# Kernel tuning notes

Hardware: AMD Instinct MI355X
Metric: run time of the kernel (lower is better)

The kernel has to match this reference:

```python
import jax, jax.numpy as jnp
import numpy as np

B, L, D = 4, 1024, 256
HD = 16                 # head_dim
H = D // HD             # num heads = 16
DI = 2 * D              # mamba d_inner (expand=2) = 512
S = 64                  # d_state
KC = 4                  # d_conv
DTR = max(1, D // 16)   # dt_rank = 16
SCALES = (1, 2, 4, 8)


def _lin_interp(x, L_out):
    # F.interpolate(mode='linear', align_corners=False) on (B, L_in, D)
    L_in = x.shape[1]
    pos = (jnp.arange(L_out, dtype=x.dtype) + 0.5) * (L_in / L_out) - 0.5
    pos = jnp.clip(pos, 0.0, L_in - 1)
    lo = jnp.floor(pos).astype(jnp.int32)
    hi = jnp.minimum(lo + 1, L_in - 1)
    w = (pos - lo.astype(x.dtype))[None, :, None]
    return x[:, lo] * (1.0 - w) + x[:, hi] * w


def setup_inputs() -> dict:
    key = jax.random.key(0)
    ks = jax.random.split(key, 24)
    sc = 0.02
    inp = {
        "x": jax.random.normal(ks[0], (B, L, D), jnp.float32),
        "ln_g": jnp.ones((D,), jnp.float32),
        "ln_b": jnp.zeros((D,), jnp.float32),
        # MultiScaleQuery: 4 per-scale projections + fuse
        "mq_w": sc * jax.random.normal(ks[1], (4, D, D), jnp.float32),
        "mq_b": sc * jax.random.normal(ks[2], (4, D), jnp.float32),
        "fuse_w": sc * jax.random.normal(ks[3], (D, 4 * D), jnp.float32),
        "fuse_b": sc * jax.random.normal(ks[4], (D,), jnp.float32),
        # Mamba params
        "in_proj_w": sc * jax.random.normal(ks[5], (2 * DI, D), jnp.float32),
        "conv_w": 0.2 * jax.random.normal(ks[6], (DI, KC), jnp.float32),
        "conv_b": sc * jax.random.normal(ks[7], (DI,), jnp.float32),
        "x_proj_w": sc * jax.random.normal(ks[8], (DTR + 2 * S, DI), jnp.float32),
        "dt_w": sc * jax.random.normal(ks[9], (DI, DTR), jnp.float32),
        "dt_b": jnp.full((DI,), -4.0, jnp.float32),  # softplus -> small dt
        "A_log": jnp.log(jnp.tile(jnp.arange(1, S + 1, dtype=jnp.float32), (DI, 1))),
        "D_ssm": jnp.ones((DI,), jnp.float32),
        "out_w": sc * jax.random.normal(ks[10], (D, DI), jnp.float32),
        # StructuredSSD (q comes from MultiScaleQuery override; q_proj unused)
        "k_w": sc * jax.random.normal(ks[11], (D, D), jnp.float32),
        "k_b": sc * jax.random.normal(ks[12], (D,), jnp.float32),
        "v_w": sc * jax.random.normal(ks[13], (D, D), jnp.float32),
        "v_b": sc * jax.random.normal(ks[14], (D,), jnp.float32),
        "o_w": sc * jax.random.normal(ks[15], (D, D), jnp.float32),
        "o_b": sc * jax.random.normal(ks[16], (D,), jnp.float32),
        "log_tau": jnp.full((H,), np.log(16.0), jnp.float32),
        # Gate
        "gate_w": sc * jax.random.normal(ks[17], (D, 2 * D), jnp.float32),
        "gate_b": sc * jax.random.normal(ks[18], (D,), jnp.float32),
    }
    return inp


def reference(x, ln_g, ln_b, mq_w, mq_b, fuse_w, fuse_b,
              in_proj_w, conv_w, conv_b, x_proj_w, dt_w, dt_b,
              A_log, D_ssm, out_w,
              k_w, k_b, v_w, v_b, o_w, o_b, log_tau,
              gate_w, gate_b):
    Bsz, Lq, Dm = x.shape

    # ---- LayerNorm ----
    mu = x.mean(-1, keepdims=True)
    var = ((x - mu) ** 2).mean(-1, keepdims=True)
    xn = (x - mu) / jnp.sqrt(var + 1e-5) * ln_g + ln_b

    # ---- MultiScaleQuery ----
    qs = []
    for i, s in enumerate(SCALES):
        if s <= 1:
            q = xn @ mq_w[i].T + mq_b[i]
        else:
            xd = xn.reshape(Bsz, Lq // s, s, Dm).mean(2)   # avg_pool1d(k=s, stride=s)
            qd = xd @ mq_w[i].T + mq_b[i]
            q = _lin_interp(qd, Lq)
        qs.append(q)
    q = jnp.concatenate(qs, -1) @ fuse_w.T + fuse_b        # (B, L, D)

    # ---- Mamba (selective scan) ----
    xz = xn @ in_proj_w.T                                  # (B, L, 2*DI)
    xm, z = jnp.split(xz, 2, axis=-1)
    xp = jnp.pad(xm, ((0, 0), (KC - 1, 0), (0, 0)))        # causal depthwise conv
    xc = sum(xp[:, kk:kk + Lq, :] * conv_w[:, kk] for kk in range(KC)) + conv_b
    xc = jax.nn.silu(xc)                                   # (B, L, DI)
    dbc = xc @ x_proj_w.T                                  # (B, L, DTR+2S)
    dt_in, Bm, Cm = jnp.split(dbc, [DTR, DTR + S], axis=-1)
    dt = jax.nn.softplus(dt_in @ dt_w.T + dt_b)            # (B, L, DI)
    A = -jnp.exp(A_log)                                    # (DI, S)

    def step(h, inp):
        xt, dtt, Bt, Ct = inp                              # (B,DI) (B,DI) (B,S) (B,S)
        dA = jnp.exp(dtt[:, :, None] * A)                  # (B, DI, S)
        h = dA * h + (dtt * xt)[:, :, None] * Bt[:, None, :]
        y = jnp.einsum('bds,bs->bd', h, Ct)
        return h, y

    h0 = jnp.zeros((Bsz, DI, S), x.dtype)
    _, ys = jax.lax.scan(step, h0, (xc.transpose(1, 0, 2), dt.transpose(1, 0, 2),
                                    Bm.transpose(1, 0, 2), Cm.transpose(1, 0, 2)))
    y = ys.transpose(1, 0, 2) + xc * D_ssm                 # (B, L, DI)
    y = y * jax.nn.silu(z)
    ssm_out = y @ out_w.T                                  # (B, L, D)

    # ---- StructuredSSD (decay-masked attention, q override) ----
    k = xn @ k_w.T + k_b
    v = xn @ v_w.T + v_b
    hds = lambda t: t.reshape(Bsz, Lq, H, HD).transpose(0, 2, 1, 3)
    qh, kh, vh = hds(q), hds(k), hds(v)                    # (B, H, L, hd)
    scale = 1.0 / np.sqrt(HD)
    scores = jnp.einsum('bhqd,bhkd->bhqk', qh, kh) * scale
    idx = jnp.arange(Lq)
    dist = jnp.maximum(idx[:, None] - idx[None, :], 0).astype(x.dtype)
    tau = jnp.exp(log_tau)[:, None, None]                  # (H,1,1)
    mask = jnp.exp(-dist / tau)                            # (H, L, L); ==1 above diag
    scores = scores * mask
    denom = jnp.maximum(mask.sum(-1, keepdims=True), 1e-6)
    scores = scores / denom                                # broadcast over batch
    attn = jnp.einsum('bhqk,bhkd->bhqd', scores, vh)
    attn = attn.transpose(0, 2, 1, 3).reshape(Bsz, Lq, Dm)
    ssd_out = attn @ o_w.T + o_b

    # ---- Sigmoid gate fusion + residual ----
    gate = jax.nn.sigmoid(jnp.concatenate([ssm_out, ssd_out], -1) @ gate_w.T + gate_b)
    fused = gate * ssm_out + (1.0 - gate) * ssd_out
    return x + fused
```

## Files before the change

kernel.cpp:

```cpp
#include <hip/hip_runtime.h>
#include <math.h>

#define Bsz 4
#define Lseq 1024
#define Dm 256
#define Hh 16
#define HDm 16
#define DIm 512
#define Ssz 64
#define KCm 4
#define DTRm 16
#define NCH (Bsz * DIm)
#define CHK 64
#define NCHK (Lseq / CHK)
#define CHA 32
#define NCA (Lseq / CHA)

typedef __attribute__((ext_vector_type(8))) short s8v;
typedef __attribute__((ext_vector_type(4))) float f4v;

static __device__ __forceinline__ float wave_sum(float v) {
    #pragma unroll
    for (int m = 32; m >= 1; m >>= 1) v += __shfl_xor(v, m, 64);
    return v;
}

static __device__ __forceinline__ float bcast(float v, int l) {
    return __uint_as_float(__builtin_amdgcn_readlane(__float_as_uint(v), l));
}

static __device__ __forceinline__ short f2bf(float f) {
    unsigned int u = __float_as_uint(f);
    u = (u + 0x7fffu + ((u >> 16) & 1u)) >> 16;
    return (short)u;
}

static __device__ __forceinline__ s8v pack8(float4 a, float4 b) {
    s8v v;
    v[0] = f2bf(a.x); v[1] = f2bf(a.y); v[2] = f2bf(a.z); v[3] = f2bf(a.w);
    v[4] = f2bf(b.x); v[5] = f2bf(b.y); v[6] = f2bf(b.z); v[7] = f2bf(b.w);
    return v;
}

__global__ __launch_bounds__(256) void ln_kernel(const float* __restrict__ x,
                                                 const float* __restrict__ g,
                                                 const float* __restrict__ b,
                                                 float* __restrict__ xn) {
    int row = blockIdx.x;
    int tid = threadIdx.x;
    __shared__ float red[8];
    float v = x[(size_t)row * Dm + tid];
    float s = wave_sum(v);
    int wid = tid >> 6, lane = tid & 63;
    if (lane == 0) red[wid] = s;
    __syncthreads();
    float mean = (red[0] + red[1] + red[2] + red[3]) * (1.0f / Dm);
    float dv = v - mean;
    float s2 = wave_sum(dv * dv);
    if (lane == 0) red[4 + wid] = s2;
    __syncthreads();
    float var = (red[4] + red[5] + red[6] + red[7]) * (1.0f / Dm);
    float inv = rsqrtf(var + 1e-5f);
    xn[(size_t)row * Dm + tid] = dv * inv * g[tid] + b[tid];
}

__global__ void halve3_kernel(const float* __restrict__ xn, float* __restrict__ xd2,
                              float* __restrict__ xd4, float* __restrict__ xd8) {
    int idx = blockIdx.x * blockDim.x + threadIdx.x;
    if (idx < 524288) {
        int d = idx & 255, j = (idx >> 8) & 511, b = idx >> 17;
        const float* p = xn + ((size_t)(b * 1024 + 2 * j) * 256 + d);
        xd2[idx] = 0.5f * (p[0] + p[256]);
    } else if (idx < 786432) {
        int i = idx - 524288;
        int d = i & 255, j = (i >> 8) & 255, b = i >> 16;
        const float* p = xn + ((size_t)(b * 1024 + 4 * j) * 256 + d);
        xd4[i] = 0.25f * ((p[0] + p[256]) + (p[512] + p[768]));
    } else if (idx < 917504) {
        int i = idx - 786432;
        int d = i & 255, j = (i >> 8) & 127, b = i >> 15;
        const float* p = xn + ((size_t)(b * 1024 + 8 * j) * 256 + d);
        xd8[i] = 0.125f * (((p[0] + p[256]) + (p[512] + p[768]))
                         + ((p[1024] + p[1280]) + (p[1536] + p[1792])));
    }
}

__global__ __launch_bounds__(256) void conv_silu_kernel(const float* __restrict__ xm,
                                                        const float* __restrict__ cw,
                                                        const float* __restrict__ cb,
                                                        float* __restrict__ xc,
                                                        float* __restrict__ xcT) {
    __shared__ float tile[64][65];
    int blk = blockIdx.x;
    int cblk = blk & 7;
    int tblk = (blk >> 3) & 15;
    int b = blk >> 7;
    int c0 = cblk * 64, t0 = tblk * 64;
    int cc = threadIdx.x & 63;
    int tw = threadIdx.x >> 6;
    int c = c0 + cc;
    float w0 = cw[c * 4 + 0], w1 = cw[c * 4 + 1], w2 = cw[c * 4 + 2], w3 = cw[c * 4 + 3];
    float bias = cb[c];
    #pragma unroll 4
    for (int i = 0; i < 16; i++) {
        int tl = tw * 16 + i;
        int t = t0 + tl;
        const float* base = xm + ((size_t)(b * Lseq + t)) * DIm + c;
        float acc = bias + base[0] * w3;
        if (t >= 3) {
            acc += base[-3 * DIm] * w0 + base[-2 * DIm] * w1 + base[-1 * DIm] * w2;
        } else {
            if (t >= 1) acc += base[-1 * DIm] * w2;
            if (t >= 2) acc += base[-2 * DIm] * w1;
        }
        float r = acc / (1.0f + __expf(-acc));
        xc[((size_t)(b * Lseq + t)) * DIm + c] = r;
        tile[tl][cc] = r;
    }
    __syncthreads();
    int tcol = threadIdx.x & 63;
    int crow0 = threadIdx.x >> 6;
    #pragma unroll 4
    for (int j = 0; j < 16; j++) {
        int crow = crow0 * 16 + j;
        xcT[((size_t)(c0 + crow)) * (Bsz * Lseq) + b * Lseq + t0 + tcol] = tile[tcol][crow];
    }
}

__global__ __launch_bounds__(256) void proj8(const float* __restrict__ xn,
                                             const float* __restrict__ xd2,
                                             const float* __restrict__ xd4,
                                             const float* __restrict__ xd8,
                                             const float* __restrict__ in_proj_w,
                                             const float* __restrict__ k_w, const float* __restrict__ k_b,
                                             const float* __restrict__ v_w, const float* __restrict__ v_b,
                                             const float* __restrict__ mq_w, const float* __restrict__ mq_b,
                                             float* __restrict__ xm, float* __restrict__ zT,
                                             float* __restrict__ kmat, float* __restrict__ vmat,
                                             float* __restrict__ q0, float* __restrict__ qd2,
                                             float* __restrict__ qd4, float* __restrict__ qd8) {
    __shared__ unsigned short As[64][40];
    __shared__ unsigned short Ws[64][40];
    int bx = blockIdx.x;
    const float* A; const float* W; const float* bias; float* C;
    int ldc, transC = 0, n0, m0;
    if (bx < 512) {
        A = xn; W = in_proj_w; bias = nullptr; C = xm; ldc = DIm;
        n0 = (bx & 7) * 64; m0 = (bx >> 3) * 64;
    } else if (bx < 1024) {
        int l = bx - 512;
        A = xn; W = in_proj_w + 131072; bias = nullptr; C = zT; ldc = Bsz * Lseq; transC = 1;
        n0 = (l & 7) * 64; m0 = (l >> 3) * 64;
    } else if (bx < 1280) {
        int l = bx - 1024;
        A = xn; W = k_w; bias = k_b; C = kmat; ldc = Dm;
        n0 = (l & 3) * 64; m0 = (l >> 2) * 64;
    } else if (bx < 1536) {
        int l = bx - 1280;
        A = xn; W = v_w; bias = v_b; C = vmat; ldc = Dm;
        n0 = (l & 3) * 64; m0 = (l >> 2) * 64;
    } else if (bx < 1792) {
        int l = bx - 1536;
        A = xn; W = mq_w; bias = mq_b; C = q0; ldc = Dm;
        n0 = (l & 3) * 64; m0 = (l >> 2) * 64;
    } else if (bx < 1920) {
        int l = bx - 1792;
        A = xd2; W = mq_w + 65536; bias = mq_b + 256; C = qd2; ldc = Dm;
        n0 = (l & 3) * 64; m0 = (l >> 2) * 64;
    } else if (bx < 1984) {
        int l = bx - 1920;
        A = xd4; W = mq_w + 131072; bias = mq_b + 512; C = qd4; ldc = Dm;
        n0 = (l & 3) * 64; m0 = (l >> 2) * 64;
    } else {
        int l = bx - 1984;
        A = xd8; W = mq_w + 196608; bias = mq_b + 768; C = qd8; ldc = Dm;
        n0 = (l & 3) * 64; m0 = (l >> 2) * 64;
    }
    int tid = threadIdx.x;
    int wave = tid >> 6, lane = tid & 63;
    int quad = lane >> 4, r = lane & 15;
    int mo = (wave >> 1) * 32, no = (wave & 1) * 32;
    f4v acc[2][2];
    #pragma unroll
    for (int i = 0; i < 2; i++)
        #pragma unroll
        for (int j = 0; j < 2; j++) acc[i][j] = (f4v){0.f, 0.f, 0.f, 0.f};
    for (int k0 = 0; k0 < 256; k0 += 32) {
        {
            int m = tid >> 2, kk = (tid & 3) * 8;
            const float* ap = A + (size_t)(m0 + m) * 256 + k0 + kk;
            *(s8v*)&As[m][kk] = pack8(*(const float4*)ap, *(const float4*)(ap + 4));
        }
        {
            int n = tid >> 2, kk = (tid & 3) * 8;
            const float* wp = W + (size_t)(n0 + n) * 256 + k0 + kk;
            *(s8v*)&Ws[n][kk] = pack8(*(const float4*)wp, *(const float4*)(wp + 4));
        }
        __syncthreads();
        s8v af[2], bf[2];
        #pragma unroll
        for (int i = 0; i < 2; i++) af[i] = *(const s8v*)&As[mo + i * 16 + r][quad * 8];
        #pragma unroll
        for (int j = 0; j < 2; j++) bf[j] = *(const s8v*)&Ws[no + j * 16 + r][quad * 8];
        #pragma unroll
        for (int i = 0; i < 2; i++)
            #pragma unroll
            for (int j = 0; j < 2; j++)
                acc[i][j] = __builtin_amdgcn_mfma_f32_16x16x32_bf16(af[i], bf[j], acc[i][j], 0, 0, 0);
        __syncthreads();
    }
    #pragma unroll
    for (int i = 0; i < 2; i++)
        #pragma unroll
        for (int j = 0; j < 2; j++)
            #pragma unroll
            for (int reg = 0; reg < 4; reg++) {
                int m = m0 + mo + i * 16 + quad * 4 + reg;
                int n = n0 + no + j * 16 + r;
                float v = acc[i][j][reg];
                if (bias) v += bias[n];
                float* cp = transC ? (C + (size_t)n * ldc + m) : (C + (size_t)m * ldc + n);
                *cp = v;
            }
}

__global__ __launch_bounds__(256) void fuse_gemm(const float* __restrict__ q0,
                                                 const float* __restrict__ qd2,
                                                 const float* __restrict__ qd4,
                                                 const float* __restrict__ qd8,
                                                 const float* __restrict__ fuse_w,
                                                 const float* __restrict__ fuse_b,
                                                 float* __restrict__ qbuf) {
    __shared__ unsigned short As[64][40];
    __shared__ unsigned short Ws[64][40];
    int tid = threadIdx.x;
    int wave = tid >> 6, lane = tid & 63;
    int quad = lane >> 4, r = lane & 15;
    int m0 = blockIdx.y * 64, n0 = blockIdx.x * 64;
    int mo = (wave >> 1) * 32, no = (wave & 1) * 32;
    f4v acc[2][2];
    #pragma unroll
    for (int i = 0; i < 2; i++)
        #pragma unroll
        for (int j = 0; j < 2; j++) acc[i][j] = (f4v){0.f, 0.f, 0.f, 0.f};

    for (int k0 = 0; k0 < 1024; k0 += 32) {
        {
            int m = tid >> 2, kk = (tid & 3) * 8;
            int kg = k0 + kk;
            int seg = kg >> 8, dcol = kg & 255;
            int mg = m0 + m;
            s8v pv;
            if (seg == 0) {
                const float* ap = q0 + (size_t)mg * 256 + dcol;
                pv = pack8(*(const float4*)ap, *(const float4*)(ap + 4));
            } else {
                int t = mg & 1023, b = mg >> 10;
                int Lin = 512 >> (seg - 1);
                const float* qd = (seg == 1) ? qd2 : (seg == 2) ? qd4 : qd8;
                float pos = (t + 0.5f) * ((float)Lin / 1024.0f) - 0.5f;
                pos = fminf(fmaxf(pos, 0.0f), (float)(Lin - 1));
                int lo = (int)floorf(pos);
                int hi = min(lo + 1, Lin - 1);
                float w = pos - (float)lo;
                const float* plo = qd + ((size_t)(b * Lin + lo)) * 256 + dcol;
                const float* phi = qd + ((size_t)(b * Lin + hi)) * 256 + dcol;
                float4 l0 = *(const float4*)plo, l1 = *(const float4*)(plo + 4);
                float4 h0 = *(const float4*)phi, h1 = *(const float4*)(phi + 4);
                float4 r0, r1;
                r0.x = l0.x + w * (h0.x - l0.x); r0.y = l0.y + w * (h0.y - l0.y);
                r0.z = l0.z + w * (h0.z - l0.z); r0.w = l0.w + w * (h0.w - l0.w);
                r1.x = l1.x + w * (h1.x - l1.x); r1.y = l1.y + w * (h1.y - l1.y);
                r1.z = l1.z + w * (h1.z - l1.z); r1.w = l1.w + w * (h1.w - l1.w);
                pv = pack8(r0, r1);
            }
            *(s8v*)&As[m][kk] = pv;
        }
        {
            int n = tid >> 2, kk = (tid & 3) * 8;
            const float* wp = fuse_w + (size_t)(n0 + n) * 1024 + k0 + kk;
            *(s8v*)&Ws[n][kk] = pack8(*(const float4*)wp, *(const float4*)(wp + 4));
        }
        __syncthreads();
        s8v af[2], bf[2];
        #pragma unroll
        for (int i = 0; i < 2; i++) af[i] = *(const s8v*)&As[mo + i * 16 + r][quad * 8];
        #pragma unroll
        for (int j = 0; j < 2; j++) bf[j] = *(const s8v*)&Ws[no + j * 16 + r][quad * 8];
        #pragma unroll
        for (int i = 0; i < 2; i++)
            #pragma unroll
            for (int j = 0; j < 2; j++)
                acc[i][j] = __builtin_amdgcn_mfma_f32_16x16x32_bf16(af[i], bf[j], acc[i][j], 0, 0, 0);
        __syncthreads();
    }
    #pragma unroll
    for (int i = 0; i < 2; i++)
        #pragma unroll
        for (int j = 0; j < 2; j++)
            #pragma unroll
            for (int reg = 0; reg < 4; reg++) {
                int m = m0 + mo + i * 16 + quad * 4 + reg;
                int n = n0 + no + j * 16 + r;
                qbuf[(size_t)m * 256 + n] = acc[i][j][reg] + fuse_b[n];
            }
}

__global__ __launch_bounds__(256) void post2(const float* __restrict__ attn,
                                             const float* __restrict__ o_w,
                                             const float* __restrict__ o_b,
                                             const float* __restrict__ yT,
                                             const float* __restrict__ out_w,
                                             float* __restrict__ cat2) {
    __shared__ unsigned short As[64][40];
    __shared__ unsigned short Ws[64][40];
    int bx = blockIdx.x;
    const float* A; const float* W; const float* bias; float* C;
    int lda_m, lda_k, ldw, K, n0, m0;
    if (bx < 256) {
        A = attn; lda_m = 256; lda_k = 1; W = o_w; ldw = 256; bias = o_b;
        C = cat2 + 256; K = 256;
        n0 = (bx & 3) * 64; m0 = (bx >> 2) * 64;
    } else {
        int l = bx - 256;
        A = yT; lda_m = 1; lda_k = Bsz * Lseq; W = out_w; ldw = DIm; bias = nullptr;
        C = cat2; K = DIm;
        n0 = (l & 3) * 64; m0 = (l >> 2) * 64;
    }
    int tid = threadIdx.x;
    int wave = tid >> 6, lane = tid & 63;
    int quad = lane >> 4, r = lane & 15;
    int mo = (wave >> 1) * 32, no = (wave & 1) * 32;
    f4v acc[2][2];
    #pragma unroll
    for (int i = 0; i < 2; i++)
        #pragma unroll
        for (int j = 0; j < 2; j++) acc[i][j] = (f4v){0.f, 0.f, 0.f, 0.f};
    for (int k0 = 0; k0 < K; k0 += 32) {
        if (lda_k == 1) {
            int m = tid >> 2, kk = (tid & 3) * 8;
            const float* ap = A + (size_t)(m0 + m) * lda_m + k0 + kk;
            *(s8v*)&As[m][kk] = pack8(*(const float4*)ap, *(const float4*)(ap + 4));
        } else {
            int k = tid >> 3, m8 = (tid & 7) * 8;
            const float* ap = A + (size_t)(k0 + k) * lda_k + m0 + m8;
            float4 a0 = *(const float4*)ap;
            float4 a1 = *(const float4*)(ap + 4);
            float av[8] = {a0.x, a0.y, a0.z, a0.w, a1.x, a1.y, a1.z, a1.w};
            #pragma unroll
            for (int i = 0; i < 8; i++) As[m8 + i][k] = (unsigned short)f2bf(av[i]);
        }
        {
            int n = tid >> 2, kk = (tid & 3) * 8;
            const float* wp = W + (size_t)(n0 + n) * ldw + k0 + kk;
            *(s8v*)&Ws[n][kk] = pack8(*(const float4*)wp, *(const float4*)(wp + 4));
        }
        __syncthreads();
        s8v af[2], bf[2];
        #pragma unroll
        for (int i = 0; i < 2; i++) af[i] = *(const s8v*)&As[mo + i * 16 + r][quad * 8];
        #pragma unroll
        for (int j = 0; j < 2; j++) bf[j] = *(const s8v*)&Ws[no + j * 16 + r][quad * 8];
        #pragma unroll
        for (int i = 0; i < 2; i++)
            #pragma unroll
            for (int j = 0; j < 2; j++)
                acc[i][j] = __builtin_amdgcn_mfma_f32_16x16x32_bf16(af[i], bf[j], acc[i][j], 0, 0, 0);
        __syncthreads();
    }
    #pragma unroll
    for (int i = 0; i < 2; i++)
        #pragma unroll
        for (int j = 0; j < 2; j++)
            #pragma unroll
            for (int reg = 0; reg < 4; reg++) {
                int m = m0 + mo + i * 16 + quad * 4 + reg;
                int n = n0 + no + j * 16 + r;
                float v = acc[i][j][reg];
                if (bias) v += bias[n];
                C[(size_t)m * 512 + n] = v;
            }
}

__global__ __launch_bounds__(256) void gemm_bf16(const float* __restrict__ A, int lda_m, int lda_k,
                                                 const float* __restrict__ W, int ldw,
                                                 const float* __restrict__ bias,
                                                 float* __restrict__ C, int ldc,
                                                 int M, int N, int K, int accum, int transC,
                                                 const float* __restrict__ xres,
                                                 float* __restrict__ fout) {
    __shared__ unsigned short As[64][40];
    __shared__ unsigned short Ws[64][40];
    int tid = threadIdx.x;
    int wave = tid >> 6, lane = tid & 63;
    int quad = lane >> 4, r = lane & 15;
    int m0 = blockIdx.y * 64, n0 = blockIdx.x * 64;
    int mo = (wave >> 1) * 32, no = (wave & 1) * 32;
    f4v acc[2][2];
    #pragma unroll
    for (int i = 0; i < 2; i++)
        #pragma unroll
        for (int j = 0; j < 2; j++) acc[i][j] = (f4v){0.f, 0.f, 0.f, 0.f};

    for (int k0 = 0; k0 < K; k0 += 32) {
        if (lda_k == 1) {
            int m = tid >> 2, kk = (tid & 3) * 8;
            const float* ap = A + (size_t)(m0 + m) * lda_m + k0 + kk;
            *(s8v*)&As[m][kk] = pack8(*(const float4*)ap, *(const float4*)(ap + 4));
        } else {
            int k = tid >> 3, m8 = (tid & 7) * 8;
            const float* ap = A + (size_t)(k0 + k) * lda_k + m0 + m8;
            float4 a0 = *(const float4*)ap;
            float4 a1 = *(const float4*)(ap + 4);
            float av[8] = {a0.x, a0.y, a0.z, a0.w, a1.x, a1.y, a1.z, a1.w};
            #pragma unroll
            for (int i = 0; i < 8; i++) As[m8 + i][k] = (unsigned short)f2bf(av[i]);
        }
        {
            int n = tid >> 2, kk = (tid & 3) * 8;
            s8v pv;
            if (n0 + n < N) {
                const float* wp = W + (size_t)(n0 + n) * ldw + k0 + kk;
                pv = pack8(*(const float4*)wp, *(const float4*)(wp + 4));
            } else {
                pv = (s8v){0, 0, 0, 0, 0, 0, 0, 0};
            }
            *(s8v*)&Ws[n][kk] = pv;
        }
        __syncthreads();
        s8v af[2], bf[2];
        #pragma unroll
        for (int i = 0; i < 2; i++) af[i] = *(const s8v*)&As[mo + i * 16 + r][quad * 8];
        #pragma unroll
        for (int j = 0; j < 2; j++) bf[j] = *(const s8v*)&Ws[no + j * 16 + r][quad * 8];
        #pragma unroll
        for (int i = 0; i < 2; i++)
            #pragma unroll
            for (int j = 0; j < 2; j++)
                acc[i][j] = __builtin_amdgcn_mfma_f32_16x16x32_bf16(af[i], bf[j], acc[i][j], 0, 0, 0);
        __syncthreads();
    }
    #pragma unroll
    for (int i = 0; i < 2; i++)
        #pragma unroll
        for (int j = 0; j < 2; j++)
            #pragma unroll
            for (int reg = 0; reg < 4; reg++) {
                int m = m0 + mo + i * 16 + quad * 4 + reg;
                int n = n0 + no + j * 16 + r;
                if (n >= N) continue;
                float v = acc[i][j][reg];
                if (bias) v += bias[n];
                if (fout) {
                    float g = 1.0f / (1.0f + __expf(-v));
                    float ssm = A[(size_t)m * lda_m + n];
                    float ssd = A[(size_t)m * lda_m + 256 + n];
                    fout[(size_t)m * 256 + n] = xres[(size_t)m * 256 + n] + g * ssm + (1.0f - g) * ssd;
                } else {
                    float* cp = transC ? (C + (size_t)n * ldc + m) : (C + (size_t)m * ldc + n);
                    if (accum) v += *cp;
                    *cp = v;
                }
            }
}

__global__ __launch_bounds__(256) void gemm_f32(const float* __restrict__ A, int lda_m, int lda_k,
                                                const float* __restrict__ W, int ldw,
                                                const float* __restrict__ bias,
                                                float* __restrict__ C, int ldc,
                                                int M, int N, int K, int act, int accum, int transC) {
    __shared__ float As[16][72];
    __shared__ float Ws[16][72];
    int tid = threadIdx.x;
    int m0 = blockIdx.y * 64, n0 = blockIdx.x * 64;
    int tx = tid & 15, ty = tid >> 4;
    float acc[4][4] = {};
    for (int k0 = 0; k0 < K; k0 += 16) {
        {
            int ml = tid >> 2, kl = (tid & 3) * 4;
            const float4 av = *(const float4*)(A + (size_t)(m0 + ml) * lda_m + k0 + kl);
            As[kl + 0][ml] = av.x; As[kl + 1][ml] = av.y;
            As[kl + 2][ml] = av.z; As[kl + 3][ml] = av.w;
        }
        {
            int nl = tid >> 2, kl = (tid & 3) * 4;
            float4 wv;
            if (n0 + nl < N) wv = *(const float4*)(W + (size_t)(n0 + nl) * ldw + k0 + kl);
            else wv = make_float4(0.f, 0.f, 0.f, 0.f);
            Ws[kl + 0][nl] = wv.x; Ws[kl + 1][nl] = wv.y;
            Ws[kl + 2][nl] = wv.z; Ws[kl + 3][nl] = wv.w;
        }
        __syncthreads();
        #pragma unroll
        for (int kk = 0; kk < 16; kk++) {
            float4 av = *(const float4*)&As[kk][ty * 4];
            float4 bv = *(const float4*)&Ws[kk][tx * 4];
            float a[4] = {av.x, av.y, av.z, av.w};
            float bb[4] = {bv.x, bv.y, bv.z, bv.w};
            #pragma unroll
            for (int im = 0; im < 4; im++)
                #pragma unroll
                for (int in = 0; in < 4; in++)
                    acc[im][in] = fmaf(a[im], bb[in], acc[im][in]);
        }
        __syncthreads();
    }
    #pragma unroll
    for (int in = 0; in < 4; in++) {
        int n = n0 + tx * 4 + in;
        if (n >= N) continue;
        #pragma unroll
        for (int im = 0; im < 4; im++) {
            int m = m0 + ty * 4 + im;
            float v = acc[im][in];
            if (bias) v += bias[n];
            if (act == 1) v = fmaxf(v, 0.0f) + log1pf(expf(-fabsf(v)));
            float* cp = transC ? (C + (size_t)n * ldc + m) : (C + (size_t)m * ldc + n);
            if (accum) v += *cp;
            *cp = v;
        }
    }
}

__global__ __launch_bounds__(256) void scan_pass1(const float* __restrict__ xcT,
                                                  const float* __restrict__ dtmT,
                                                  const float* __restrict__ dbc,
                                                  const float* __restrict__ A_log,
                                                  float* __restrict__ hloc,
                                                  float* __restrict__ Pc) {
    int wave = blockIdx.x * 4 + (threadIdx.x >> 6);
    int lane = threadIdx.x & 63;
    int ch = wave & (NCH - 1);
    int c  = wave >> 11;
    int b = ch >> 9, d = ch & (DIm - 1);
    float As = -__expf(A_log[d * Ssz + lane]);
    int base_m = b * Lseq + c * CHK;
    float dt_vec = dtmT[(size_t)d * (Bsz * Lseq) + base_m + lane];
    float x_vec  = xcT [(size_t)d * (Bsz * Lseq) + base_m + lane];
    float ux = dt_vec * x_vec;
    float S = dt_vec;
    #pragma unroll
    for (int m = 1; m < 64; m <<= 1) {
        float o = __shfl_up(S, m, 64);
        if (lane >= m) S += o;
    }
    float Stot = bcast(S, 63);
    const float* Bp = dbc + (size_t)base_m * 144 + DTRm + lane;
    float h0 = 0.f, h1 = 0.f, h2 = 0.f, h3 = 0.f;
    #pragma unroll 4
    for (int t = 0; t < CHK; t += 4) {
        float B0 = Bp[0], B1 = Bp[144], B2 = Bp[288], B3 = Bp[432];
        Bp += 576;
        float w0 = __expf(As * (Stot - bcast(S, t)))     * bcast(ux, t);
        float w1 = __expf(As * (Stot - bcast(S, t + 1))) * bcast(ux, t + 1);
        float w2 = __expf(As * (Stot - bcast(S, t + 2))) * bcast(ux, t + 2);
        float w3 = __expf(As * (Stot - bcast(S, t + 3))) * bcast(ux, t + 3);
        h0 = fmaf(w0, B0, h0); h1 = fmaf(w1, B1, h1);
        h2 = fmaf(w2, B2, h2); h3 = fmaf(w3, B3, h3);
    }
    size_t o = ((size_t)ch * NCHK + c) * Ssz + lane;
    hloc[o] = (h0 + h1) + (h2 + h3);
    Pc[o] = __expf(As * Stot);
}

__global__ __launch_bounds__(256) void scan_combine(const float* __restrict__ hloc,
                                                    const float* __restrict__ Pc,
                                                    float* __restrict__ Hinit) {
    int wave = blockIdx.x * 4 + (threadIdx.x >> 6);
    int lane = threadIdx.x & 63;
    size_t base = (size_t)wave * NCHK * Ssz + lane;
    float H = 0.0f;
    #pragma unroll
    for (int c = 0; c < NCHK; c++) {
        size_t o = base + (size_t)c * Ssz;
        Hinit[o] = H;
        H = fmaf(Pc[o], H, hloc[o]);
    }
}

__global__ __launch_bounds__(256) void scan_pass3(const float* __restrict__ xcT,
                                                  const float* __restrict__ dtmT,
                                                  const float* __restrict__ zT,
                                                  const float* __restrict__ dbc,
                                                  const float* __restrict__ A_log,
                                                  const float* __restrict__ D_ssm,
                                                  const float* __restrict__ Hinit,
                                                  float* __restrict__ yT) {
    __shared__ float hCs[4][16][68];
    int wid = threadIdx.x >> 6;
    int lane = threadIdx.x & 63;
    int wave = blockIdx.x * 4 + wid;
    int ch = wave & (NCH - 1);
    int c  = wave >> 11;
    int b = ch >> 9, d = ch & (DIm - 1);
    float As = -__expf(A_log[d * Ssz + lane]);
    float Dd = D_ssm[d];
    int base_m = b * Lseq + c * CHK;
    float dt_vec = dtmT[(size_t)d * (Bsz * Lseq) + base_m + lane];
    float x_vec  = xcT [(size_t)d * (Bsz * Lseq) + base_m + lane];
    float zown   = zT  [(size_t)d * (Bsz * Lseq) + base_m + lane];
    float ux = dt_vec * x_vec;
    const float* Bp = dbc + (size_t)base_m * 144 + DTRm + lane;
    const float* Cp = Bp + Ssz;
    float h = Hinit[((size_t)ch * NCHK + c) * Ssz + lane];
    float yred = 0.0f;
    int tl = lane >> 2;
    int so = (lane & 3) * 16;
    for (int tb = 0; tb < 4; tb++) {
        #pragma unroll
        for (int j = 0; j < 16; j++) {
            int t = tb * 16 + j;
            float Bt = *Bp; Bp += 144;
            float Ct = *Cp; Cp += 144;
            float dtv = bcast(dt_vec, t);
            float u   = bcast(ux, t);
            float dA = __expf(dtv * As);
            h = fmaf(dA, h, u * Bt);
            hCs[wid][j][lane] = h * Ct;
        }
        const float* bp = &hCs[wid][tl][so];
        float4 a0 = *(const float4*)(bp + 0);
        float4 a1 = *(const float4*)(bp + 4);
        float4 a2 = *(const float4*)(bp + 8);
        float4 a3 = *(const float4*)(bp + 12);
        float part = ((a0.x + a0.y) + (a0.z + a0.w)) + ((a1.x + a1.y) + (a1.z + a1.w))
                   + ((a2.x + a2.y) + (a2.z + a2.w)) + ((a3.x + a3.y) + (a3.z + a3.w));
        part += __shfl_xor(part, 1, 64);
        part += __shfl_xor(part, 2, 64);
        float got = __shfl(part, ((lane - tb * 16) << 2) & 63, 64);
        if ((lane >> 4) == tb) yred = got;
    }
    float yg = (yred + x_vec * Dd) * (zown / (1.0f + __expf(-zown)));
    yT[(size_t)d * (Bsz * Lseq) + base_m + lane] = yg;
}

__global__ __launch_bounds__(256) void attn_p1(const float* __restrict__ k,
                                               const float* __restrict__ v,
                                               const float* __restrict__ log_tau,
                                               float* __restrict__ loc) {
    __shared__ float Ksh[4][CHA][20];
    __shared__ float Vsh[4][CHA][16];
    int wid = threadIdx.x >> 6, lane = threadIdx.x & 63;
    int wave = blockIdx.x * 4 + wid;
    int bh = wave >> 5;
    int c  = wave & 31;
    int b = bh >> 4, h = bh & 15;
    float inv_tau = __expf(-log_tau[h]);
    float rdec = __expf(-inv_tau);
    int t0 = c * CHA;
    int row = lane >> 1, hf = (lane & 1) * 8;
    const float* kp = k + ((size_t)(b * Lseq + t0 + row)) * Dm + h * HDm + hf;
    const float* vp = v + ((size_t)(b * Lseq + t0 + row)) * Dm + h * HDm + hf;
    *(float4*)&Ksh[wid][row][hf]     = *(const float4*)kp;
    *(float4*)&Ksh[wid][row][hf + 4] = *(const float4*)(kp + 4);
    *(float4*)&Vsh[wid][row][hf]     = *(const float4*)vp;
    *(float4*)&Vsh[wid][row][hf + 4] = *(const float4*)(vp + 4);
    int g = lane >> 4, cc = lane & 15;
    float4 U = {0.f, 0.f, 0.f, 0.f}, T = {0.f, 0.f, 0.f, 0.f};
    #pragma unroll 8
    for (int s = 0; s < CHA; s++) {
        float4 kf = *(const float4*)&Ksh[wid][s][4 * g];
        float vv = Vsh[wid][s][cc];
        float u0 = kf.x * vv, u1 = kf.y * vv, u2 = kf.z * vv, u3 = kf.w * vv;
        U.x += u0; U.y += u1; U.z += u2; U.w += u3;
        T.x = fmaf(rdec, T.x, u0); T.y = fmaf(rdec, T.y, u1);
        T.z = fmaf(rdec, T.z, u2); T.w = fmaf(rdec, T.w, u3);
    }
    float* op = loc + ((size_t)bh * NCA + c) * 512;
    *(float4*)(op + lane * 4) = U;
    *(float4*)(op + 256 + lane * 4) = T;
}

__global__ __launch_bounds__(256) void attn_p2(const float* __restrict__ loc,
                                               const float* __restrict__ log_tau,
                                               float* __restrict__ init,
                                               float* __restrict__ kvtot) {
    int bh = blockIdx.x, e = threadIdx.x;
    float inv_tau = __expf(-log_tau[bh & 15]);
    float rp = __expf(-(float)CHA * inv_tau);
    const float* lp = loc + (size_t)bh * NCA * 512;
    float* ip = init + (size_t)bh * NCA * 512;
    float Ua = 0.f, Ta = 0.f;
    #pragma unroll 8
    for (int c = 0; c < NCA; c++) {
        ip[c * 512 + e] = Ua;
        Ua += lp[c * 512 + e];
        ip[c * 512 + 256 + e] = Ta;
        Ta = fmaf(rp, Ta, lp[c * 512 + 256 + e]);
    }
    kvtot[bh * 256 + e] = Ua;
}

__global__ __launch_bounds__(256) void attn_p3(const float* __restrict__ q,
                                               const float* __restrict__ k,
                                               const float* __restrict__ v,
                                               const float* __restrict__ log_tau,
                                               const float* __restrict__ init,
                                               const float* __restrict__ kvtot,
                                               float* __restrict__ out) {
    __shared__ float Ksh[4][CHA][20];
    __shared__ float Qsh[4][CHA][20];
    __shared__ float Vsh[4][CHA][16];
    __shared__ float Ysh[4][CHA][16];
    int wid = threadIdx.x >> 6, lane = threadIdx.x & 63;
    int wave = blockIdx.x * 4 + wid;
    int bh = wave >> 5;
    int c  = wave & 31;
    int b = bh >> 4, h = bh & 15;
    float inv_tau = __expf(-log_tau[h]);
    float rdec = __expf(-inv_tau);
    int t0 = c * CHA;
    int row = lane >> 1, hf = (lane & 1) * 8;
    const float* kp = k + ((size_t)(b * Lseq + t0 + row)) * Dm + h * HDm + hf;
    const float* vp = v + ((size_t)(b * Lseq + t0 + row)) * Dm + h * HDm + hf;
    const float* qp = q + ((size_t)(b * Lseq + t0 + row)) * Dm + h * HDm + hf;
    *(float4*)&Ksh[wid][row][hf]     = *(const float4*)kp;
    *(float4*)&Ksh[wid][row][hf + 4] = *(const float4*)(kp + 4);
    *(float4*)&Vsh[wid][row][hf]     = *(const float4*)vp;
    *(float4*)&Vsh[wid][row][hf + 4] = *(const float4*)(vp + 4);
    *(float4*)&Qsh[wid][row][hf]     = *(const float4*)qp;
    *(float4*)&Qsh[wid][row][hf + 4] = *(const float4*)(qp + 4);
    int g = lane >> 4, cc = lane & 15;
    size_t ibase = ((size_t)bh * NCA + c) * 512;
    float4 U  = *(const float4*)(init + ibase + lane * 4);
    float4 T  = *(const float4*)(init + ibase + 256 + lane * 4);
    float4 KV = *(const float4*)(kvtot + bh * 256 + lane * 4);
    float om = 1.0f - rdec;
    float geom = (om > 1e-8f) ? (1.0f - __expf(-inv_tau * (float)t0)) / om : (float)t0;
    #pragma unroll 4
    for (int s = 0; s < CHA; s++) {
        int i = t0 + s;
        geom = fmaf(geom, rdec, 1.0f);
        float4 kf = *(const float4*)&Ksh[wid][s][4 * g];
        float4 qf = *(const float4*)&Qsh[wid][s][4 * g];
        float vv = Vsh[wid][s][cc];
        float u0 = kf.x * vv, u1 = kf.y * vv, u2 = kf.z * vv, u3 = kf.w * vv;
        U.x += u0; U.y += u1; U.z += u2; U.w += u3;
        T.x = fmaf(rdec, T.x, u0); T.y = fmaf(rdec, T.y, u1);
        T.z = fmaf(rdec, T.z, u2); T.w = fmaf(rdec, T.w, u3);
        float p;
        p = qf.x * (KV.x - U.x + T.x);
        p = fmaf(qf.y, KV.y - U.y + T.y, p);
        p = fmaf(qf.z, KV.z - U.z + T.z, p);
        p = fmaf(qf.w, KV.w - U.w + T.w, p);
        p += __shfl_xor(p, 16, 64);
        p += __shfl_xor(p, 32, 64);
        float deno = fmaxf((float)(Lseq - 1 - i) + geom, 1e-6f);
        float yv = p * (0.25f / deno);
        if (lane < 16) Ysh[wid][s][lane] = yv;
    }
    float* op = out + ((size_t)(b * Lseq + t0 + row)) * Dm + h * HDm + hf;
    *(float4*)op       = *(const float4*)&Ysh[wid][row][hf];
    *(float4*)(op + 4) = *(const float4*)&Ysh[wid][row][hf + 4];
}

extern "C" void kernel_launch(void* const* d_in, const int* in_sizes, int n_in,
                              void* d_out, int out_size, void* d_ws, size_t ws_size,
                              hipStream_t stream) {
    const float* x        = (const float*)d_in[0];
    const float* ln_g     = (const float*)d_in[1];
    const float* ln_b     = (const float*)d_in[2];
    const float* mq_w     = (const float*)d_in[3];
    const float* mq_b     = (const float*)d_in[4];
    const float* fuse_w   = (const float*)d_in[5];
    const float* fuse_b   = (const float*)d_in[6];
    const float* in_proj_w= (const float*)d_in[7];
    const float* conv_w   = (const float*)d_in[8];
    const float* conv_b   = (const float*)d_in[9];
    const float* x_proj_w = (const float*)d_in[10];
    const float* dt_w     = (const float*)d_in[11];
    const float* dt_b     = (const float*)d_in[12];
    const float* A_log    = (const float*)d_in[13];
    const float* D_ssm    = (const float*)d_in[14];
    const float* out_w    = (const float*)d_in[15];
    const float* k_w      = (const float*)d_in[16];
    const float* k_b      = (const float*)d_in[17];
    const float* v_w      = (const float*)d_in[18];
    const float* v_b      = (const float*)d_in[19];
    const float* o_w      = (const float*)d_in[20];
    const float* o_b      = (const float*)d_in[21];
    const float* log_tau  = (const float*)d_in[22];
    const float* gate_w   = (const float*)d_in[23];
    const float* gate_b   = (const float*)d_in[24];
    float* outp = (float*)d_out;

    const int M = Bsz * Lseq;
    float* ws = (float*)d_ws;
    size_t off = 0;
    float* xn    = ws + off; off += (size_t)M * Dm;
    float* xm    = ws + off; off += (size_t)M * DIm;
    float* zT    = ws + off; off += (size_t)DIm * M;
    float* xcT   = ws + off; off += (size_t)DIm * M;
    float* dbc   = ws + off; off += (size_t)M * 144;
    float* dtmT  = ws + off; off += (size_t)DIm * M;
    float* yT    = ws + off; off += (size_t)DIm * M;
    float* xd2   = ws + off; off += (size_t)Bsz * 512 * Dm;
    float* xd4   = ws + off; off += (size_t)Bsz * 256 * Dm;
    float* xd8   = ws + off; off += (size_t)Bsz * 128 * Dm;
    float* qd2   = ws + off; off += (size_t)Bsz * 512 * Dm;
    float* qd4   = ws + off; off += (size_t)Bsz * 256 * Dm;
    float* qd8   = ws + off; off += (size_t)Bsz * 128 * Dm;
    float* qcat  = ws + off; off += (size_t)M * 4 * Dm;
    float* qbuf  = ws + off; off += (size_t)M * Dm;
    float* kmat  = ws + off; off += (size_t)M * Dm;
    float* vmat  = ws + off; off += (size_t)M * Dm;
    float* attn  = ws + off; off += (size_t)M * Dm;
    float* cat2  = ws + off; off += (size_t)M * 2 * Dm;
    float* xc    = cat2;
    float* q0    = qcat;

    ln_kernel<<<M, 256, 0, stream>>>(x, ln_g, ln_b, xn);

    halve3_kernel<<<(917504 + 255) / 256, 256, 0, stream>>>(xn, xd2, xd4, xd8);

    proj8<<<2016, 256, 0, stream>>>(xn, xd2, xd4, xd8, in_proj_w,
        k_w, k_b, v_w, v_b, mq_w, mq_b,
        xm, zT, kmat, vmat, q0, qd2, qd4, qd8);

    fuse_gemm<<<dim3(4, 64), 256, 0, stream>>>(q0, qd2, qd4, qd8, fuse_w, fuse_b, qbuf);

    conv_silu_kernel<<<512, 256, 0, stream>>>(xm, conv_w, conv_b, xc, xcT);

    gemm_bf16<<<dim3(3, 64), 256, 0, stream>>>(xc, DIm, 1, x_proj_w, DIm,
        nullptr, dbc, 144, M, 144, DIm, 0, 0, nullptr, nullptr);

    gemm_f32<<<dim3(8, 64), 256, 0, stream>>>(dbc, 144, 1, dt_w, DTRm,
        dt_b, dtmT, M, M, DIm, DTRm, 1, 0, 1);

    float* aloc  = qcat;
    float* ainit = qcat + (size_t)64 * NCA * 512;
    float* kvtot = qcat + (size_t)2 * 64 * NCA * 512;
    attn_p1<<<512, 256, 0, stream>>>(kmat, vmat, log_tau, aloc);
    attn_p2<<<64, 256, 0, stream>>>(aloc, log_tau, ainit, kvtot);
    attn_p3<<<512, 256, 0, stream>>>(qbuf, kmat, vmat, log_tau, ainit, kvtot, attn);

    float* hloc  = qcat;
    float* Pc    = qcat + (size_t)NCH * NCHK * Ssz;
    float* Hinit = qbuf;
    scan_pass1<<<(NCH * NCHK) / 4, 256, 0, stream>>>(xcT, dtmT, dbc, A_log, hloc, Pc);
    scan_combine<<<NCH / 4, 256, 0, stream>>>(hloc, Pc, Hinit);
    scan_pass3<<<(NCH * NCHK) / 4, 256, 0, stream>>>(xcT, dtmT, zT, dbc, A_log, D_ssm, Hinit, yT);

    post2<<<512, 256, 0, stream>>>(attn, o_w, o_b, yT, out_w, cat2);

    gemm_bf16<<<dim3(4, 64), 256, 0, stream>>>(cat2, 2 * Dm, 1, gate_w, 2 * Dm,
        gate_b, nullptr, 0, M, Dm, 2 * Dm, 0, 0, x, outp);
}
```

Before: 365.0 us.

## Merge independent stages into horizontally fused kernels to cut launches

Fuses layernorm with multiscale average pooling in one kernel. It then packs independent stages into shared launches by block-index ranges: fuse GEMM with conv+SiLU, x_proj GEMM with attention pass 1, dt GEMM with attention pass 2, and scan pass 1 with attention pass 3. The attention chunk size is halved and the scan combine writes back in place. The aim is fewer kernel launches and better overlap of small independent stages, at the cost of heterogeneous blocks inside each kernel and reused workspace aliasing that must stay race-free.

```diff
diff --git a/kernel.cpp b/kernel.cpp
--- a/kernel.cpp
+++ b/kernel.cpp
@@ -13,7 +13,7 @@
 #define NCH (Bsz * DIm)
 #define CHK 64
 #define NCHK (Lseq / CHK)
-#define CHA 32
+#define CHA 16
 #define NCA (Lseq / CHA)
 
 typedef __attribute__((ext_vector_type(8))) short s8v;
@@ -42,88 +42,57 @@
     return v;
 }
 
-__global__ __launch_bounds__(256) void ln_kernel(const float* __restrict__ x,
-                                                 const float* __restrict__ g,
-                                                 const float* __restrict__ b,
-                                                 float* __restrict__ xn) {
-    int row = blockIdx.x;
-    int tid = threadIdx.x;
-    __shared__ float red[8];
-    float v = x[(size_t)row * Dm + tid];
-    float s = wave_sum(v);
-    int wid = tid >> 6, lane = tid & 63;
-    if (lane == 0) red[wid] = s;
+__global__ __launch_bounds__(256) void ln_pool(const float* __restrict__ x,
+                                               const float* __restrict__ g,
+                                               const float* __restrict__ bb,
+                                               float* __restrict__ xn, float* __restrict__ xd2,
+                                               float* __restrict__ xd4, float* __restrict__ xd8) {
+    __shared__ float p2[4][256];
+    int wid = threadIdx.x >> 6, lane = threadIdx.x & 63;
+    int gr0 = blockIdx.x * 8;
+    int b = gr0 >> 10, t0 = gr0 & 1023;
+    float4 g4 = *(const float4*)(g + lane * 4);
+    float4 b4 = *(const float4*)(bb + lane * 4);
+    float4 res[2];
+    #pragma unroll
+    for (int rr = 0; rr < 2; rr++) {
+        int row = gr0 + wid * 2 + rr;
+        float4 xv = *(const float4*)(x + (size_t)row * 256 + lane * 4);
+        float s = wave_sum(xv.x + xv.y + xv.z + xv.w);
+        float mean = s * (1.0f / 256.0f);
+        float d0 = xv.x - mean, d1 = xv.y - mean, d2 = xv.z - mean, d3 = xv.w - mean;
+        float s2 = wave_sum(d0 * d0 + d1 * d1 + d2 * d2 + d3 * d3);
+        float inv = rsqrtf(s2 * (1.0f / 256.0f) + 1e-5f);
+        float4 r;
+        r.x = d0 * inv * g4.x + b4.x; r.y = d1 * inv * g4.y + b4.y;
+        r.z = d2 * inv * g4.z + b4.z; r.w = d3 * inv * g4.w + b4.w;
+        *(float4*)(xn + (size_t)row * 256 + lane * 4) = r;
+        res[rr] = r;
+    }
+    float4 a2;
+    a2.x = 0.5f * (res[0].x + res[1].x); a2.y = 0.5f * (res[0].y + res[1].y);
+    a2.z = 0.5f * (res[0].z + res[1].z); a2.w = 0.5f * (res[0].w + res[1].w);
+    *(float4*)(xd2 + (size_t)(b * 512 + (t0 >> 1) + wid) * 256 + lane * 4) = a2;
+    *(float4*)&p2[wid][lane * 4] = a2;
     __syncthreads();
-    float mean = (red[0] + red[1] + red[2] + red[3]) * (1.0f / Dm);
-    float dv = v - mean;
-    float s2 = wave_sum(dv * dv);
-    if (lane == 0) red[4 + wid] = s2;
-    __syncthreads();
-    float var = (red[4] + red[5] + red[6] + red[7]) * (1.0f / Dm);
-    float inv = rsqrtf(var + 1e-5f);
-    xn[(size_t)row * Dm + tid] = dv * inv * g[tid] + b[tid];
-}
-
-__global__ void halve3_kernel(const float* __restrict__ xn, float* __restrict__ xd2,
-                              float* __restrict__ xd4, float* __restrict__ xd8) {
-    int idx = blockIdx.x * blockDim.x + threadIdx.x;
-    if (idx < 524288) {
-        int d = idx & 255, j = (idx >> 8) & 511, b = idx >> 17;
-        const float* p = xn + ((size_t)(b * 1024 + 2 * j) * 256 + d);
-        xd2[idx] = 0.5f * (p[0] + p[256]);
-    } else if (idx < 786432) {
-        int i = idx - 524288;
-        int d = i & 255, j = (i >> 8) & 255, b = i >> 16;
-        const float* p = xn + ((size_t)(b * 1024 + 4 * j) * 256 + d);
-        xd4[i] = 0.25f * ((p[0] + p[256]) + (p[512] + p[768]));
-    } else if (idx < 917504) {
-        int i = idx - 786432;
-        int d = i & 255, j = (i >> 8) & 127, b = i >> 15;
-        const float* p = xn + ((size_t)(b * 1024 + 8 * j) * 256 + d);
-        xd8[i] = 0.125f * (((p[0] + p[256]) + (p[512] + p[768]))
-                         + ((p[1024] + p[1280]) + (p[1536] + p[1792])));
-    }
-}
-
-__global__ __launch_bounds__(256) void conv_silu_kernel(const float* __restrict__ xm,
-                                                        const float* __restrict__ cw,
-                                                        const float* __restrict__ cb,
-                                                        float* __restrict__ xc,
-                                                        float* __restrict__ xcT) {
-    __shared__ float tile[64][65];
-    int blk = blockIdx.x;
-    int cblk = blk & 7;
-    int tblk = (blk >> 3) & 15;
-    int b = blk >> 7;
-    int c0 = cblk * 64, t0 = tblk * 64;
-    int cc = threadIdx.x & 63;
-    int tw = threadIdx.x >> 6;
-    int c = c0 + cc;
-    float w0 = cw[c * 4 + 0], w1 = cw[c * 4 + 1], w2 = cw[c * 4 + 2], w3 = cw[c * 4 + 3];
-    float bias = cb[c];
-    #pragma unroll 4
-    for (int i = 0; i < 16; i++) {
-        int tl = tw * 16 + i;
-        int t = t0 + tl;
-        const float* base = xm + ((size_t)(b * Lseq + t)) * DIm + c;
-        float acc = bias + base[0] * w3;
-        if (t >= 3) {
-            acc += base[-3 * DIm] * w0 + base[-2 * DIm] * w1 + base[-1 * DIm] * w2;
-        } else {
-            if (t >= 1) acc += base[-1 * DIm] * w2;
-            if (t >= 2) acc += base[-2 * DIm] * w1;
-        }
-        float r = acc / (1.0f + __expf(-acc));
-        xc[((size_t)(b * Lseq + t)) * DIm + c] = r;
-        tile[tl][cc] = r;
-    }
-    __syncthreads();
-    int tcol = threadIdx.x & 63;
-    int crow0 = threadIdx.x >> 6;
-    #pragma unroll 4
-    for (int j = 0; j < 16; j++) {
-        int crow = crow0 * 16 + j;
-        xcT[((size_t)(c0 + crow)) * (Bsz * Lseq) + b * Lseq + t0 + tcol] = tile[tcol][crow];
+    if (wid < 2) {
+        float4 u = *(const float4*)&p2[2 * wid][lane * 4];
+        float4 w = *(const float4*)&p2[2 * wid + 1][lane * 4];
+        float4 m;
+        m.x = 0.5f * (u.x + w.x); m.y = 0.5f * (u.y + w.y);
+        m.z = 0.5f * (u.z + w.z); m.w = 0.5f * (u.w + w.w);
+        *(float4*)(xd4 + (size_t)(b * 256 + (t0 >> 2) + wid) * 256 + lane * 4) = m;
+    } else if (wid == 2) {
+        float4 q0 = *(const float4*)&p2[0][lane * 4];
+        float4 q1 = *(const float4*)&p2[1][lane * 4];
+        float4 q2 = *(const float4*)&p2[2][lane * 4];
+        float4 q3 = *(const float4*)&p2[3][lane * 4];
+        float4 m;
+        m.x = 0.25f * ((q0.x + q1.x) + (q2.x + q3.x));
+        m.y = 0.25f * ((q0.y + q1.y) + (q2.y + q3.y));
+        m.z = 0.25f * ((q0.z + q1.z) + (q2.z + q3.z));
+        m.w = 0.25f * ((q0.w + q1.w) + (q2.w + q3.w));
+        *(float4*)(xd8 + (size_t)(b * 128 + (t0 >> 3)) * 256 + lane * 4) = m;
     }
 }
 
@@ -224,269 +193,250 @@
             }
 }
 
-__global__ __launch_bounds__(256) void fuse_gemm(const float* __restrict__ q0,
-                                                 const float* __restrict__ qd2,
-                                                 const float* __restrict__ qd4,
-                                                 const float* __restrict__ qd8,
-                                                 const float* __restrict__ fuse_w,
-                                                 const float* __restrict__ fuse_b,
-                                                 float* __restrict__ qbuf) {
-    __shared__ unsigned short As[64][40];
-    __shared__ unsigned short Ws[64][40];
+__global__ __launch_bounds__(256) void mid2(const float* __restrict__ q0,
+                                            const float* __restrict__ qd2,
+                                            const float* __restrict__ qd4,
+                                            const float* __restrict__ qd8,
+                                            const float* __restrict__ fuse_w,
+                                            const float* __restrict__ fuse_b,
+                                            float* __restrict__ qbuf,
+                                            const float* __restrict__ xm,
+                                            const float* __restrict__ cw,
+                                            const float* __restrict__ cb,
+                                            float* __restrict__ xc, float* __restrict__ xcT) {
+    __shared__ __align__(16) char smem[16640];
+    int bx = blockIdx.x;
     int tid = threadIdx.x;
-    int wave = tid >> 6, lane = tid & 63;
-    int quad = lane >> 4, r = lane & 15;
-    int m0 = blockIdx.y * 64, n0 = blockIdx.x * 64;
-    int mo = (wave >> 1) * 32, no = (wave & 1) * 32;
-    f4v acc[2][2];
-    #pragma unroll
-    for (int i = 0; i < 2; i++)
-        #pragma unroll
-        for (int j = 0; j < 2; j++) acc[i][j] = (f4v){0.f, 0.f, 0.f, 0.f};
-
-    for (int k0 = 0; k0 < 1024; k0 += 32) {
-        {
-            int m = tid >> 2, kk = (tid & 3) * 8;
-            int kg = k0 + kk;
-            int seg = kg >> 8, dcol = kg & 255;
-            int mg = m0 + m;
-            s8v pv;
-            if (seg == 0) {
-                const float* ap = q0 + (size_t)mg * 256 + dcol;
-                pv = pack8(*(const float4*)ap, *(const float4*)(ap + 4));
+    if (bx < 256) {
+        unsigned short (*As)[40] = (unsigned short(*)[40])smem;
+        unsigned short (*Ws)[40] = (unsigned short(*)[40])(smem + 5120);
+        int wave = tid >> 6, lane = tid & 63;
+        int quad = lane >> 4, r = lane & 15;
+        int n0 = (bx & 3) * 64, m0 = (bx >> 2) * 64;
+        int mo = (wave >> 1) * 32, no = (wave & 1) * 32;
+        f4v acc[2][2];
+        #pragma unroll
+        for (int i = 0; i < 2; i++)
+            #pragma unroll
+            for (int j = 0; j < 2; j++) acc[i][j] = (f4v){0.f, 0.f, 0.f, 0.f};
+        for (int k0 = 0; k0 < 1024; k0 += 32) {
+            {
+                int m = tid >> 2, kk = (tid & 3) * 8;
+                int kg = k0 + kk;
+                int seg = kg >> 8, dcol = kg & 255;
+                int mg = m0 + m;
+                s8v pv;
+                if (seg == 0) {
+                    const float* ap = q0 + (size_t)mg * 256 + dcol;
+                    pv = pack8(*(const float4*)ap, *(const float4*)(ap + 4));
+                } else {
+                    int t = mg & 1023, b = mg >> 10;
+                    int Lin = 512 >> (seg - 1);
+                    const float* qd = (seg == 1) ? qd2 : (seg == 2) ? qd4 : qd8;
+                    float pos = (t + 0.5f) * ((float)Lin / 1024.0f) - 0.5f;
+                    pos = fminf(fmaxf(pos, 0.0f), (float)(Lin - 1));
+                    int lo = (int)floorf(pos);
+                    int hi = min(lo + 1, Lin - 1);
+                    float w = pos - (float)lo;
+                    const float* plo = qd + ((size_t)(b * Lin + lo)) * 256 + dcol;
+                    const float* phi = qd + ((size_t)(b * Lin + hi)) * 256 + dcol;
+                    float4 l0 = *(const float4*)plo, l1 = *(const float4*)(plo + 4);
+                    float4 h0 = *(const float4*)phi, h1 = *(const float4*)(phi + 4);
+                    float4 r0, r1;
+                    r0.x = l0.x + w * (h0.x - l0.x); r0.y = l0.y + w * (h0.y - l0.y);
+                    r0.z = l0.z + w * (h0.z - l0.z); r0.w = l0.w + w * (h0.w - l0.w);
+                    r1.x = l1.x + w * (h1.x - l1.x); r1.y = l1.y + w * (h1.y - l1.y);
+                    r1.z = l1.z + w * (h1.z - l1.z); r1.w = l1.w + w * (h1.w - l1.w);
+                    pv = pack8(r0, r1);
+                }
+                *(s8v*)&As[m][kk] = pv;
+            }
+            {
+                int n = tid >> 2, kk = (tid & 3) * 8;
+                const float* wp = fuse_w + (size_t)(n0 + n) * 1024 + k0 + kk;
+                *(s8v*)&Ws[n][kk] = pack8(*(const float4*)wp, *(const float4*)(wp + 4));
+            }
+            __syncthreads();
+            s8v af[2], bf[2];
+            #pragma unroll
+            for (int i = 0; i < 2; i++) af[i] = *(const s8v*)&As[mo + i * 16 + r][quad * 8];
+            #pragma unroll
+            for (int j = 0; j < 2; j++) bf[j] = *(const s8v*)&Ws[no + j * 16 + r][quad * 8];
+            #pragma unroll
+            for (int i = 0; i < 2; i++)
+                #pragma unroll
+                for (int j = 0; j < 2; j++)
+                    acc[i][j] = __builtin_amdgcn_mfma_f32_16x16x32_bf16(af[i], bf[j], acc[i][j], 0, 0, 0);
+            __syncthreads();
+        }
+        #pragma unroll
+        for (int i = 0; i < 2; i++)
+            #pragma unroll
+            for (int j = 0; j < 2; j++)
+                #pragma unroll
+                for (int reg = 0; reg < 4; reg++) {
+                    int m = m0 + mo + i * 16 + quad * 4 + reg;
+                    int n = n0 + no + j * 16 + r;
+                    qbuf[(size_t)m * 256 + n] = acc[i][j][reg] + fuse_b[n];
+                }
+    } else {
+        float (*tile)[65] = (float(*)[65])smem;
+        int blk = bx - 256;
+        int cblk = blk & 7;
+        int tblk = (blk >> 3) & 15;
+        int b = blk >> 7;
+        int c0 = cblk * 64, t0 = tblk * 64;
+        int cc = tid & 63;
+        int tw = tid >> 6;
+        int c = c0 + cc;
+        float w0 = cw[c * 4 + 0], w1 = cw[c * 4 + 1], w2 = cw[c * 4 + 2], w3 = cw[c * 4 + 3];
+        float bias = cb[c];
+        #pragma unroll 4
+        for (int i = 0; i < 16; i++) {
+            int tl = tw * 16 + i;
+            int t = t0 + tl;
+            const float* base = xm + ((size_t)(b * Lseq + t)) * DIm + c;
+            float acc = bias + base[0] * w3;
+            if (t >= 3) {
+                acc += base[-3 * DIm] * w0 + base[-2 * DIm] * w1 + base[-1 * DIm] * w2;
             } else {
-                int t = mg & 1023, b = mg >> 10;
-                int Lin = 512 >> (seg - 1);
-                const float* qd = (seg == 1) ? qd2 : (seg == 2) ? qd4 : qd8;
-                float pos = (t + 0.5f) * ((float)Lin / 1024.0f) - 0.5f;
-                pos = fminf(fmaxf(pos, 0.0f), (float)(Lin - 1));
-                int lo = (int)floorf(pos);
-                int hi = min(lo + 1, Lin - 1);
-                float w = pos - (float)lo;
-                const float* plo = qd + ((size_t)(b * Lin + lo)) * 256 + dcol;
-                const float* phi = qd + ((size_t)(b * Lin + hi)) * 256 + dcol;
-                float4 l0 = *(const float4*)plo, l1 = *(const float4*)(plo + 4);
-                float4 h0 = *(const float4*)phi, h1 = *(const float4*)(phi + 4);
-                float4 r0, r1;
-                r0.x = l0.x + w * (h0.x - l0.x); r0.y = l0.y + w * (h0.y - l0.y);
-                r0.z = l0.z + w * (h0.z - l0.z); r0.w = l0.w + w * (h0.w - l0.w);
-                r1.x = l1.x + w * (h1.x - l1.x); r1.y = l1.y + w * (h1.y - l1.y);
-                r1.z = l1.z + w * (h1.z - l1.z); r1.w = l1.w + w * (h1.w - l1.w);
-                pv = pack8(r0, r1);
+                if (t >= 1) acc += base[-1 * DIm] * w2;
+                if (t >= 2) acc += base[-2 * DIm] * w1;
             }
-            *(s8v*)&As[m][kk] = pv;
-        }
-        {
-            int n = tid >> 2, kk = (tid & 3) * 8;
-            const float* wp = fuse_w + (size_t)(n0 + n) * 1024 + k0 + kk;
-            *(s8v*)&Ws[n][kk] = pack8(*(const float4*)wp, *(const float4*)(wp + 4));
+            float r = acc / (1.0f + __expf(-acc));
+            xc[((size_t)(b * Lseq + t)) * DIm + c] = r;
+            tile[tl][cc] = r;
         }
         __syncthreads();
-        s8v af[2], bf[2];
-        #pragma unroll
-        for (int i = 0; i < 2; i++) af[i] = *(const s8v*)&As[mo + i * 16 + r][quad * 8];
-        #pragma unroll
-        for (int j = 0; j < 2; j++) bf[j] = *(const s8v*)&Ws[no + j * 16 + r][quad * 8];
+        int tcol = tid & 63;
+        int crow0 = tid >> 6;
+        #pragma unroll 4
+        for (int j = 0; j < 16; j++) {
+            int crow = crow0 * 16 + j;
+            xcT[((size_t)(c0 + crow)) * (Bsz * Lseq) + b * Lseq + t0 + tcol] = tile[tcol][crow];
+        }
+    }
+}
+
+__global__ __launch_bounds__(256) void xproj_ap1(const float* __restrict__ xc,
+                                                 const float* __restrict__ x_proj_w,
+                                                 float* __restrict__ dbc,
+                                                 const float* __restrict__ kmat,
+                                                 const float* __restrict__ vmat,
+                                                 const float* __restrict__ log_tau,
+                                                 float* __restrict__ loc) {
+    __shared__ __align__(16) char smem[10240];
+    int bx = blockIdx.x;
+    int tid = threadIdx.x;
+    int wid = tid >> 6, lane = tid & 63;
+    if (bx < 192) {
+        unsigned short (*As)[40] = (unsigned short(*)[40])smem;
+        unsigned short (*Ws)[40] = (unsigned short(*)[40])(smem + 5120);
+        int quad = lane >> 4, r = lane & 15;
+        int n0 = (bx % 3) * 64, m0 = (bx / 3) * 64;
+        int mo = (wid >> 1) * 32, no = (wid & 1) * 32;
+        f4v acc[2][2];
         #pragma unroll
         for (int i = 0; i < 2; i++)
             #pragma unroll
+            for (int j = 0; j < 2; j++) acc[i][j] = (f4v){0.f, 0.f, 0.f, 0.f};
+        for (int k0 = 0; k0 < 512; k0 += 32) {
+            {
+                int m = tid >> 2, kk = (tid & 3) * 8;
+                const float* ap = xc + (size_t)(m0 + m) * 512 + k0 + kk;
+                *(s8v*)&As[m][kk] = pack8(*(const float4*)ap, *(const float4*)(ap + 4));
+            }
+            {
+                int n = tid >> 2, kk = (tid & 3) * 8;
+                s8v pv;
+                if (n0 + n < 144) {
+                    const float* wp = x_proj_w + (size_t)(n0 + n) * 512 + k0 + kk;
+                    pv = pack8(*(const float4*)wp, *(const float4*)(wp + 4));
+                } else {
+                    pv = (s8v){0, 0, 0, 0, 0, 0, 0, 0};
+                }
+                *(s8v*)&Ws[n][kk] = pv;
+            }
+            __syncthreads();
+            s8v af[2], bf[2];
+            #pragma unroll
+            for (int i = 0; i < 2; i++) af[i] = *(const s8v*)&As[mo + i * 16 + r][quad * 8];
+            #pragma unroll
+            for (int j = 0; j < 2; j++) bf[j] = *(const s8v*)&Ws[no + j * 16 + r][quad * 8];
+            #pragma unroll
+            for (int i = 0; i < 2; i++)
+                #pragma unroll
+                for (int j = 0; j < 2; j++)
+                    acc[i][j] = __builtin_amdgcn_mfma_f32_16x16x32_bf16(af[i], bf[j], acc[i][j], 0, 0, 0);
+            __syncthreads();
+        }
+        #pragma unroll
+        for (int i = 0; i < 2; i++)
+            #pragma unroll
             for (int j = 0; j < 2; j++)
-                acc[i][j] = __builtin_amdgcn_mfma_f32_16x16x32_bf16(af[i], bf[j], acc[i][j], 0, 0, 0);
-        __syncthreads();
-    }
-    #pragma unroll
-    for (int i = 0; i < 2; i++)
-        #pragma unroll
-        for (int j = 0; j < 2; j++)
-            #pragma unroll
-            for (int reg = 0; reg < 4; reg++) {
-                int m = m0 + mo + i * 16 + quad * 4 + reg;
-                int n = n0 + no + j * 16 + r;
-                qbuf[(size_t)m * 256 + n] = acc[i][j][reg] + fuse_b[n];
-            }
-}
-
-__global__ __launch_bounds__(256) void post2(const float* __restrict__ attn,
-                                             const float* __restrict__ o_w,
-                                             const float* __restrict__ o_b,
-                                             const float* __restrict__ yT,
-                                             const float* __restrict__ out_w,
-                                             float* __restrict__ cat2) {
-    __shared__ unsigned short As[64][40];
-    __shared__ unsigned short Ws[64][40];
+                #pragma unroll
+                for (int reg = 0; reg < 4; reg++) {
+                    int m = m0 + mo + i * 16 + quad * 4 + reg;
+                    int n = n0 + no + j * 16 + r;
+                    if (n >= 144) continue;
+                    dbc[(size_t)m * 144 + n] = acc[i][j][reg];
+                }
+    } else {
+        float (*Ksh)[CHA][20] = (float(*)[CHA][20])smem;
+        float (*Vsh)[CHA][16] = (float(*)[CHA][16])(smem + 5120);
+        int wv = (bx - 192) * 4 + wid;
+        int bh = wv >> 6, c = wv & 63;
+        int b = bh >> 4, h = bh & 15;
+        float inv_tau = __expf(-log_tau[h]);
+        float rdec = __expf(-inv_tau);
+        int t0 = c * CHA;
+        int row = lane >> 2, q4 = (lane & 3) * 4;
+        const float* kp = kmat + ((size_t)(b * Lseq + t0 + row)) * Dm + h * HDm + q4;
+        const float* vp = vmat + ((size_t)(b * Lseq + t0 + row)) * Dm + h * HDm + q4;
+        *(float4*)&Ksh[wid][row][q4] = *(const float4*)kp;
+        *(float4*)&Vsh[wid][row][q4] = *(const float4*)vp;
+        int g = lane >> 4, cc = lane & 15;
+        float4 U = {0.f, 0.f, 0.f, 0.f}, T = {0.f, 0.f, 0.f, 0.f};
+        #pragma unroll
+        for (int s = 0; s < CHA; s++) {
+            float4 kf = *(const float4*)&Ksh[wid][s][4 * g];
+            float vv = Vsh[wid][s][cc];
+            float u0 = kf.x * vv, u1 = kf.y * vv, u2 = kf.z * vv, u3 = kf.w * vv;
+            U.x += u0; U.y += u1; U.z += u2; U.w += u3;
+            T.x = fmaf(rdec, T.x, u0); T.y = fmaf(rdec, T.y, u1);
+            T.z = fmaf(rdec, T.z, u2); T.w = fmaf(rdec, T.w, u3);
+        }
+        float* op = loc + ((size_t)bh * NCA + c) * 512;
+        *(float4*)(op + lane * 4) = U;
+        *(float4*)(op + 256 + lane * 4) = T;
+    }
+}
+
+__global__ __launch_bounds__(256) void dt_ap2(const float* __restrict__ dbc,
+                                              const float* __restrict__ dt_w,
+                                              const float* __restrict__ dt_b,
+                                              float* __restrict__ dtmT,
+                                              float* __restrict__ loc,
+                                              const float* __restrict__ log_tau,
+                                              float* __restrict__ kvtot) {
+    __shared__ __align__(16) char smem[9216];
     int bx = blockIdx.x;
-    const float* A; const float* W; const float* bias; float* C;
-    int lda_m, lda_k, ldw, K, n0, m0;
-    if (bx < 256) {
-        A = attn; lda_m = 256; lda_k = 1; W = o_w; ldw = 256; bias = o_b;
-        C = cat2 + 256; K = 256;
-        n0 = (bx & 3) * 64; m0 = (bx >> 2) * 64;
-    } else {
-        int l = bx - 256;
-        A = yT; lda_m = 1; lda_k = Bsz * Lseq; W = out_w; ldw = DIm; bias = nullptr;
-        C = cat2; K = DIm;
-        n0 = (l & 3) * 64; m0 = (l >> 2) * 64;
-    }
     int tid = threadIdx.x;
-    int wave = tid >> 6, lane = tid & 63;
-    int quad = lane >> 4, r = lane & 15;
-    int mo = (wave >> 1) * 32, no = (wave & 1) * 32;
-    f4v acc[2][2];
-    #pragma unroll
-    for (int i = 0; i < 2; i++)
-        #pragma unroll
-        for (int j = 0; j < 2; j++) acc[i][j] = (f4v){0.f, 0.f, 0.f, 0.f};
-    for (int k0 = 0; k0 < K; k0 += 32) {
-        if (lda_k == 1) {
-            int m = tid >> 2, kk = (tid & 3) * 8;
-            const float* ap = A + (size_t)(m0 + m) * lda_m + k0 + kk;
-            *(s8v*)&As[m][kk] = pack8(*(const float4*)ap, *(const float4*)(ap + 4));
-        } else {
-            int k = tid >> 3, m8 = (tid & 7) * 8;
-            const float* ap = A + (size_t)(k0 + k) * lda_k + m0 + m8;
-            float4 a0 = *(const float4*)ap;
-            float4 a1 = *(const float4*)(ap + 4);
-            float av[8] = {a0.x, a0.y, a0.z, a0.w, a1.x, a1.y, a1.z, a1.w};
-            #pragma unroll
-            for (int i = 0; i < 8; i++) As[m8 + i][k] = (unsigned short)f2bf(av[i]);
-        }
-        {
-            int n = tid >> 2, kk = (tid & 3) * 8;
-            const float* wp = W + (size_t)(n0 + n) * ldw + k0 + kk;
-            *(s8v*)&Ws[n][kk] = pack8(*(const float4*)wp, *(const float4*)(wp + 4));
-        }
-        __syncthreads();
-        s8v af[2], bf[2];
-        #pragma unroll
-        for (int i = 0; i < 2; i++) af[i] = *(const s8v*)&As[mo + i * 16 + r][quad * 8];
-        #pragma unroll
-        for (int j = 0; j < 2; j++) bf[j] = *(const s8v*)&Ws[no + j * 16 + r][quad * 8];
-        #pragma unroll
-        for (int i = 0; i < 2; i++)
-            #pragma unroll
-            for (int j = 0; j < 2; j++)
-                acc[i][j] = __builtin_amdgcn_mfma_f32_16x16x32_bf16(af[i], bf[j], acc[i][j], 0, 0, 0);
-        __syncthreads();
-    }
-    #pragma unroll
-    for (int i = 0; i < 2; i++)
-        #pragma unroll
-        for (int j = 0; j < 2; j++)
-            #pragma unroll
-            for (int reg = 0; reg < 4; reg++) {
-                int m = m0 + mo + i * 16 + quad * 4 + reg;
-                int n = n0 + no + j * 16 + r;
-                float v = acc[i][j][reg];
-                if (bias) v += bias[n];
-                C[(size_t)m * 512 + n] = v;
-            }
-}
-
-__global__ __launch_bounds__(256) void gemm_bf16(const float* __restrict__ A, int lda_m, int lda_k,
-                                                 const float* __restrict__ W, int ldw,
-                                                 const float* __restrict__ bias,
-                                                 float* __restrict__ C, int ldc,
-                                                 int M, int N, int K, int accum, int transC,
-                                                 const float* __restrict__ xres,
-                                                 float* __restrict__ fout) {
-    __shared__ unsigned short As[64][40];
-    __shared__ unsigned short Ws[64][40];
-    int tid = threadIdx.x;
-    int wave = tid >> 6, lane = tid & 63;
-    int quad = lane >> 4, r = lane & 15;
-    int m0 = blockIdx.y * 64, n0 = blockIdx.x * 64;
-    int mo = (wave >> 1) * 32, no = (wave & 1) * 32;
-    f4v acc[2][2];
-    #pragma unroll
-    for (int i = 0; i < 2; i++)
-        #pragma unroll
-        for (int j = 0; j < 2; j++) acc[i][j] = (f4v){0.f, 0.f, 0.f, 0.f};
-
-    for (int k0 = 0; k0 < K; k0 += 32) {
-        if (lda_k == 1) {
-            int m = tid >> 2, kk = (tid & 3) * 8;
-            const float* ap = A + (size_t)(m0 + m) * lda_m + k0 + kk;
-            *(s8v*)&As[m][kk] = pack8(*(const float4*)ap, *(const float4*)(ap + 4));
-        } else {
-            int k = tid >> 3, m8 = (tid & 7) * 8;
-            const float* ap = A + (size_t)(k0 + k) * lda_k + m0 + m8;
-            float4 a0 = *(const float4*)ap;
-            float4 a1 = *(const float4*)(ap + 4);
-            float av[8] = {a0.x, a0.y, a0.z, a0.w, a1.x, a1.y, a1.z, a1.w};
-            #pragma unroll
-            for (int i = 0; i < 8; i++) As[m8 + i][k] = (unsigned short)f2bf(av[i]);
-        }
-        {
-            int n = tid >> 2, kk = (tid & 3) * 8;
-            s8v pv;
-            if (n0 + n < N) {
-                const float* wp = W + (size_t)(n0 + n) * ldw + k0 + kk;
-                pv = pack8(*(const float4*)wp, *(const float4*)(wp + 4));
-            } else {
-                pv = (s8v){0, 0, 0, 0, 0, 0, 0, 0};
-            }
-            *(s8v*)&Ws[n][kk] = pv;
-        }
-        __syncthreads();
-        s8v af[2], bf[2];
-        #pragma unroll
-        for (int i = 0; i < 2; i++) af[i] = *(const s8v*)&As[mo + i * 16 + r][quad * 8];
-        #pragma unroll
-        for (int j = 0; j < 2; j++) bf[j] = *(const s8v*)&Ws[no + j * 16 + r][quad * 8];
-        #pragma unroll
-        for (int i = 0; i < 2; i++)
-            #pragma unroll
-            for (int j = 0; j < 2; j++)
-                acc[i][j] = __builtin_amdgcn_mfma_f32_16x16x32_bf16(af[i], bf[j], acc[i][j], 0, 0, 0);
-        __syncthreads();
-    }
-    #pragma unroll
-    for (int i = 0; i < 2; i++)
-        #pragma unroll
-        for (int j = 0; j < 2; j++)
-            #pragma unroll
-            for (int reg = 0; reg < 4; reg++) {
-                int m = m0 + mo + i * 16 + quad * 4 + reg;
-                int n = n0 + no + j * 16 + r;
-                if (n >= N) continue;
-                float v = acc[i][j][reg];
-                if (bias) v += bias[n];
-                if (fout) {
-                    float g = 1.0f / (1.0f + __expf(-v));
-                    float ssm = A[(size_t)m * lda_m + n];
-                    float ssd = A[(size_t)m * lda_m + 256 + n];
-                    fout[(size_t)m * 256 + n] = xres[(size_t)m * 256 + n] + g * ssm + (1.0f - g) * ssd;
-                } else {
-                    float* cp = transC ? (C + (size_t)n * ldc + m) : (C + (size_t)m * ldc + n);
-                    if (accum) v += *cp;
-                    *cp = v;
-                }
-            }
-}
-
-__global__ __launch_bounds__(256) void gemm_f32(const float* __restrict__ A, int lda_m, int lda_k,
-                                                const float* __restrict__ W, int ldw,
-                                                const float* __restrict__ bias,
-                                                float* __restrict__ C, int ldc,
-                                                int M, int N, int K, int act, int accum, int transC) {
-    __shared__ float As[16][72];
-    __shared__ float Ws[16][72];
-    int tid = threadIdx.x;
-    int m0 = blockIdx.y * 64, n0 = blockIdx.x * 64;
-    int tx = tid & 15, ty = tid >> 4;
-    float acc[4][4] = {};
-    for (int k0 = 0; k0 < K; k0 += 16) {
+    if (bx < 512) {
+        float (*As)[72] = (float(*)[72])smem;
+        float (*Ws)[72] = (float(*)[72])(smem + 4608);
+        int m0 = (bx >> 3) * 64, n0 = (bx & 7) * 64;
+        int tx = tid & 15, ty = tid >> 4;
+        float acc[4][4] = {};
         {
             int ml = tid >> 2, kl = (tid & 3) * 4;
-            const float4 av = *(const float4*)(A + (size_t)(m0 + ml) * lda_m + k0 + kl);
+            const float4 av = *(const float4*)(dbc + (size_t)(m0 + ml) * 144 + kl);
             As[kl + 0][ml] = av.x; As[kl + 1][ml] = av.y;
             As[kl + 2][ml] = av.z; As[kl + 3][ml] = av.w;
         }
         {
             int nl = tid >> 2, kl = (tid & 3) * 4;
-            float4 wv;
-            if (n0 + nl < N) wv = *(const float4*)(W + (size_t)(n0 + nl) * ldw + k0 + kl);
-            else wv = make_float4(0.f, 0.f, 0.f, 0.f);
+            float4 wv = *(const float4*)(dt_w + (size_t)(n0 + nl) * 16 + kl);
             Ws[kl + 0][nl] = wv.x; Ws[kl + 1][nl] = wv.y;
             Ws[kl + 2][nl] = wv.z; Ws[kl + 3][nl] = wv.w;
         }
@@ -496,76 +446,147 @@
             float4 av = *(const float4*)&As[kk][ty * 4];
             float4 bv = *(const float4*)&Ws[kk][tx * 4];
             float a[4] = {av.x, av.y, av.z, av.w};
-            float bb[4] = {bv.x, bv.y, bv.z, bv.w};
+            float bbv[4] = {bv.x, bv.y, bv.z, bv.w};
             #pragma unroll
             for (int im = 0; im < 4; im++)
                 #pragma unroll
                 for (int in = 0; in < 4; in++)
-                    acc[im][in] = fmaf(a[im], bb[in], acc[im][in]);
-        }
-        __syncthreads();
-    }
-    #pragma unroll
-    for (int in = 0; in < 4; in++) {
-        int n = n0 + tx * 4 + in;
-        if (n >= N) continue;
-        #pragma unroll
-        for (int im = 0; im < 4; im++) {
-            int m = m0 + ty * 4 + im;
-            float v = acc[im][in];
-            if (bias) v += bias[n];
-            if (act == 1) v = fmaxf(v, 0.0f) + log1pf(expf(-fabsf(v)));
-            float* cp = transC ? (C + (size_t)n * ldc + m) : (C + (size_t)m * ldc + n);
-            if (accum) v += *cp;
-            *cp = v;
-        }
-    }
-}
-
-__global__ __launch_bounds__(256) void scan_pass1(const float* __restrict__ xcT,
-                                                  const float* __restrict__ dtmT,
-                                                  const float* __restrict__ dbc,
-                                                  const float* __restrict__ A_log,
-                                                  float* __restrict__ hloc,
-                                                  float* __restrict__ Pc) {
-    int wave = blockIdx.x * 4 + (threadIdx.x >> 6);
-    int lane = threadIdx.x & 63;
-    int ch = wave & (NCH - 1);
-    int c  = wave >> 11;
-    int b = ch >> 9, d = ch & (DIm - 1);
-    float As = -__expf(A_log[d * Ssz + lane]);
-    int base_m = b * Lseq + c * CHK;
-    float dt_vec = dtmT[(size_t)d * (Bsz * Lseq) + base_m + lane];
-    float x_vec  = xcT [(size_t)d * (Bsz * Lseq) + base_m + lane];
-    float ux = dt_vec * x_vec;
-    float S = dt_vec;
-    #pragma unroll
-    for (int m = 1; m < 64; m <<= 1) {
-        float o = __shfl_up(S, m, 64);
-        if (lane >= m) S += o;
-    }
-    float Stot = bcast(S, 63);
-    const float* Bp = dbc + (size_t)base_m * 144 + DTRm + lane;
-    float h0 = 0.f, h1 = 0.f, h2 = 0.f, h3 = 0.f;
-    #pragma unroll 4
-    for (int t = 0; t < CHK; t += 4) {
-        float B0 = Bp[0], B1 = Bp[144], B2 = Bp[288], B3 = Bp[432];
-        Bp += 576;
-        float w0 = __expf(As * (Stot - bcast(S, t)))     * bcast(ux, t);
-        float w1 = __expf(As * (Stot - bcast(S, t + 1))) * bcast(ux, t + 1);
-        float w2 = __expf(As * (Stot - bcast(S, t + 2))) * bcast(ux, t + 2);
-        float w3 = __expf(As * (Stot - bcast(S, t + 3))) * bcast(ux, t + 3);
-        h0 = fmaf(w0, B0, h0); h1 = fmaf(w1, B1, h1);
-        h2 = fmaf(w2, B2, h2); h3 = fmaf(w3, B3, h3);
-    }
-    size_t o = ((size_t)ch * NCHK + c) * Ssz + lane;
-    hloc[o] = (h0 + h1) + (h2 + h3);
-    Pc[o] = __expf(As * Stot);
-}
-
-__global__ __launch_bounds__(256) void scan_combine(const float* __restrict__ hloc,
-                                                    const float* __restrict__ Pc,
-                                                    float* __restrict__ Hinit) {
+                    acc[im][in] = fmaf(a[im], bbv[in], acc[im][in]);
+        }
+        #pragma unroll
+        for (int in = 0; in < 4; in++) {
+            int n = n0 + tx * 4 + in;
+            #pragma unroll
+            for (int im = 0; im < 4; im++) {
+                int m = m0 + ty * 4 + im;
+                float v = acc[im][in] + dt_b[n];
+                v = fmaxf(v, 0.0f) + log1pf(expf(-fabsf(v)));
+                dtmT[(size_t)n * (Bsz * Lseq) + m] = v;
+            }
+        }
+    } else {
+        int bh = bx - 512, e = tid;
+        float inv_tau = __expf(-log_tau[bh & 15]);
+        float rp = __expf(-(float)CHA * inv_tau);
+        float* lp = loc + (size_t)bh * NCA * 512;
+        float Ua = 0.f, Ta = 0.f;
+        #pragma unroll 8
+        for (int c = 0; c < NCA; c++) {
+            float tu = lp[c * 512 + e];
+            lp[c * 512 + e] = Ua;
+            Ua += tu;
+            float tt = lp[c * 512 + 256 + e];
+            lp[c * 512 + 256 + e] = Ta;
+            Ta = fmaf(rp, Ta, tt);
+        }
+        kvtot[bh * 256 + e] = Ua;
+    }
+}
+
+__global__ __launch_bounds__(256) void sp1_ap3(const float* __restrict__ xcT,
+                                               const float* __restrict__ dtmT,
+                                               const float* __restrict__ dbc,
+                                               const float* __restrict__ A_log,
+                                               float* __restrict__ hloc,
+                                               float* __restrict__ Pc,
+                                               const float* __restrict__ q,
+                                               const float* __restrict__ kmat,
+                                               const float* __restrict__ vmat,
+                                               const float* __restrict__ log_tau,
+                                               const float* __restrict__ init,
+                                               const float* __restrict__ kvtot,
+                                               float* __restrict__ attn_out) {
+    __shared__ __align__(16) char smem[18432];
+    int bx = blockIdx.x;
+    int tid = threadIdx.x;
+    int wid = tid >> 6, lane = tid & 63;
+    if (bx < 8192) {
+        int wave = bx * 4 + wid;
+        int ch = wave & (NCH - 1);
+        int c  = wave >> 11;
+        int b = ch >> 9, d = ch & (DIm - 1);
+        float As = -__expf(A_log[d * Ssz + lane]);
+        int base_m = b * Lseq + c * CHK;
+        float dt_vec = dtmT[(size_t)d * (Bsz * Lseq) + base_m + lane];
+        float x_vec  = xcT [(size_t)d * (Bsz * Lseq) + base_m + lane];
+        float ux = dt_vec * x_vec;
+        float S = dt_vec;
+        #pragma unroll
+        for (int m = 1; m < 64; m <<= 1) {
+            float o = __shfl_up(S, m, 64);
+            if (lane >= m) S += o;
+        }
+        float Stot = bcast(S, 63);
+        const float* Bp = dbc + (size_t)base_m * 144 + DTRm + lane;
+        float h0 = 0.f, h1 = 0.f, h2 = 0.f, h3 = 0.f;
+        #pragma unroll 4
+        for (int t = 0; t < CHK; t += 4) {
+            float B0 = Bp[0], B1 = Bp[144], B2 = Bp[288], B3 = Bp[432];
+            Bp += 576;
+            float w0 = __expf(As * (Stot - bcast(S, t)))     * bcast(ux, t);
+            float w1 = __expf(As * (Stot - bcast(S, t + 1))) * bcast(ux, t + 1);
+            float w2 = __expf(As * (Stot - bcast(S, t + 2))) * bcast(ux, t + 2);
+            float w3 = __expf(As * (Stot - bcast(S, t + 3))) * bcast(ux, t + 3);
+            h0 = fmaf(w0, B0, h0); h1 = fmaf(w1, B1, h1);
+            h2 = fmaf(w2, B2, h2); h3 = fmaf(w3, B3, h3);
+        }
+        size_t o = ((size_t)ch * NCHK + c) * Ssz + lane;
+        hloc[o] = (h0 + h1) + (h2 + h3);
+        Pc[o] = __expf(As * Stot);
+    } else {
+        float (*Ksh)[CHA][20] = (float(*)[CHA][20])smem;
+        float (*Qsh)[CHA][20] = (float(*)[CHA][20])(smem + 5120);
+        float (*Vsh)[CHA][16] = (float(*)[CHA][16])(smem + 10240);
+        float (*Ysh)[CHA][16] = (float(*)[CHA][16])(smem + 14336);
+        int wv = (bx - 8192) * 4 + wid;
+        int bh = wv >> 6, c = wv & 63;
+        int b = bh >> 4, h = bh & 15;
+        float inv_tau = __expf(-log_tau[h]);
+        float rdec = __expf(-inv_tau);
+        int t0 = c * CHA;
+        int row = lane >> 2, q4 = (lane & 3) * 4;
+        const float* kp = kmat + ((size_t)(b * Lseq + t0 + row)) * Dm + h * HDm + q4;
+        const float* vp = vmat + ((size_t)(b * Lseq + t0 + row)) * Dm + h * HDm + q4;
+        const float* qp = q    + ((size_t)(b * Lseq + t0 + row)) * Dm + h * HDm + q4;
+        *(float4*)&Ksh[wid][row][q4] = *(const float4*)kp;
+        *(float4*)&Vsh[wid][row][q4] = *(const float4*)vp;
+        *(float4*)&Qsh[wid][row][q4] = *(const float4*)qp;
+        int g = lane >> 4, cc = lane & 15;
+        size_t ibase = ((size_t)bh * NCA + c) * 512;
+        float4 U  = *(const float4*)(init + ibase + lane * 4);
+        float4 T  = *(const float4*)(init + ibase + 256 + lane * 4);
+        float4 KV = *(const float4*)(kvtot + bh * 256 + lane * 4);
+        float om = 1.0f - rdec;
+        float geom = (om > 1e-8f) ? (1.0f - __expf(-inv_tau * (float)t0)) / om : (float)t0;
+        #pragma unroll
+        for (int s = 0; s < CHA; s++) {
+            int i = t0 + s;
+            geom = fmaf(geom, rdec, 1.0f);
+            float4 kf = *(const float4*)&Ksh[wid][s][4 * g];
+            float4 qf = *(const float4*)&Qsh[wid][s][4 * g];
+            float vv = Vsh[wid][s][cc];
+            float u0 = kf.x * vv, u1 = kf.y * vv, u2 = kf.z * vv, u3 = kf.w * vv;
+            U.x += u0; U.y += u1; U.z += u2; U.w += u3;
+            T.x = fmaf(rdec, T.x, u0); T.y = fmaf(rdec, T.y, u1);
+            T.z = fmaf(rdec, T.z, u2); T.w = fmaf(rdec, T.w, u3);
+            float p;
+            p = qf.x * (KV.x - U.x + T.x);
+            p = fmaf(qf.y, KV.y - U.y + T.y, p);
+            p = fmaf(qf.z, KV.z - U.z + T.z, p);
+            p = fmaf(qf.w, KV.w - U.w + T.w, p);
+            p += __shfl_xor(p, 16, 64);
+            p += __shfl_xor(p, 32, 64);
+            float deno = fmaxf((float)(Lseq - 1 - i) + geom, 1e-6f);
+            float yv = p * (0.25f / deno);
+            if (lane < 16) Ysh[wid][s][lane] = yv;
+        }
+        float* op = attn_out + ((size_t)(b * Lseq + t0 + row)) * Dm + h * HDm + q4;
+        *(float4*)op = *(const float4*)&Ysh[wid][row][q4];
+    }
+}
+
+__global__ __launch_bounds__(256) void scan_combine(float* __restrict__ hloc,
+                                                    const float* __restrict__ Pc) {
     int wave = blockIdx.x * 4 + (threadIdx.x >> 6);
     int lane = threadIdx.x & 63;
     size_t base = (size_t)wave * NCHK * Ssz + lane;
@@ -573,8 +594,10 @@
     #pragma unroll
     for (int c = 0; c < NCHK; c++) {
         size_t o = base + (size_t)c * Ssz;
-        Hinit[o] = H;
-        H = fmaf(Pc[o], H, hloc[o]);
+        float p = Pc[o];
+        float hl = hloc[o];
+        hloc[o] = H;
+        H = fmaf(p, H, hl);
     }
 }
 
@@ -634,124 +657,137 @@
     yT[(size_t)d * (Bsz * Lseq) + base_m + lane] = yg;
 }
 
-__global__ __launch_bounds__(256) void attn_p1(const float* __restrict__ k,
-                                               const float* __restrict__ v,
-                                               const float* __restrict__ log_tau,
-                                               float* __restrict__ loc) {
-    __shared__ float Ksh[4][CHA][20];
-    __shared__ float Vsh[4][CHA][16];
-    int wid = threadIdx.x >> 6, lane = threadIdx.x & 63;
-    int wave = blockIdx.x * 4 + wid;
-    int bh = wave >> 5;
-    int c  = wave & 31;
-    int b = bh >> 4, h = bh & 15;
-    float inv_tau = __expf(-log_tau[h]);
-    float rdec = __expf(-inv_tau);
-    int t0 = c * CHA;
-    int row = lane >> 1, hf = (lane & 1) * 8;
-    const float* kp = k + ((size_t)(b * Lseq + t0 + row)) * Dm + h * HDm + hf;
-    const float* vp = v + ((size_t)(b * Lseq + t0 + row)) * Dm + h * HDm + hf;
-    *(float4*)&Ksh[wid][row][hf]     = *(const float4*)kp;
-    *(float4*)&Ksh[wid][row][hf + 4] = *(const float4*)(kp + 4);
-    *(float4*)&Vsh[wid][row][hf]     = *(const float4*)vp;
-    *(float4*)&Vsh[wid][row][hf + 4] = *(const float4*)(vp + 4);
-    int g = lane >> 4, cc = lane & 15;
-    float4 U = {0.f, 0.f, 0.f, 0.f}, T = {0.f, 0.f, 0.f, 0.f};
-    #pragma unroll 8
-    for (int s = 0; s < CHA; s++) {
-        float4 kf = *(const float4*)&Ksh[wid][s][4 * g];
-        float vv = Vsh[wid][s][cc];
-        float u0 = kf.x * vv, u1 = kf.y * vv, u2 = kf.z * vv, u3 = kf.w * vv;
-        U.x += u0; U.y += u1; U.z += u2; U.w += u3;
-        T.x = fmaf(rdec, T.x, u0); T.y = fmaf(rdec, T.y, u1);
-        T.z = fmaf(rdec, T.z, u2); T.w = fmaf(rdec, T.w, u3);
-    }
-    float* op = loc + ((size_t)bh * NCA + c) * 512;
-    *(float4*)(op + lane * 4) = U;
-    *(float4*)(op + 256 + lane * 4) = T;
-}
-
-__global__ __launch_bounds__(256) void attn_p2(const float* __restrict__ loc,
-                                               const float* __restrict__ log_tau,
-                                               float* __restrict__ init,
-                                               float* __restrict__ kvtot) {
-    int bh = blockIdx.x, e = threadIdx.x;
-    float inv_tau = __expf(-log_tau[bh & 15]);
-    float rp = __expf(-(float)CHA * inv_tau);
-    const float* lp = loc + (size_t)bh * NCA * 512;
-    float* ip = init + (size_t)bh * NCA * 512;
-    float Ua = 0.f, Ta = 0.f;
-    #pragma unroll 8
-    for (int c = 0; c < NCA; c++) {
-        ip[c * 512 + e] = Ua;
-        Ua += lp[c * 512 + e];
-        ip[c * 512 + 256 + e] = Ta;
-        Ta = fmaf(rp, Ta, lp[c * 512 + 256 + e]);
-    }
-    kvtot[bh * 256 + e] = Ua;
-}
-
-__global__ __launch_bounds__(256) void attn_p3(const float* __restrict__ q,
-                                               const float* __restrict__ k,
-                                               const float* __restrict__ v,
-                                               const float* __restrict__ log_tau,
-                                               const float* __restrict__ init,
-                                               const float* __restrict__ kvtot,
-                                               float* __restrict__ out) {
-    __shared__ float Ksh[4][CHA][20];
-    __shared__ float Qsh[4][CHA][20];
-    __shared__ float Vsh[4][CHA][16];
-    __shared__ float Ysh[4][CHA][16];
-    int wid = threadIdx.x >> 6, lane = threadIdx.x & 63;
-    int wave = blockIdx.x * 4 + wid;
-    int bh = wave >> 5;
-    int c  = wave & 31;
-    int b = bh >> 4, h = bh & 15;
-    float inv_tau = __expf(-log_tau[h]);
-    float rdec = __expf(-inv_tau);
-    int t0 = c * CHA;
-    int row = lane >> 1, hf = (lane & 1) * 8;
-    const float* kp = k + ((size_t)(b * Lseq + t0 + row)) * Dm + h * HDm + hf;
-    const float* vp = v + ((size_t)(b * Lseq + t0 + row)) * Dm + h * HDm + hf;
-    const float* qp = q + ((size_t)(b * Lseq + t0 + row)) * Dm + h * HDm + hf;
-    *(float4*)&Ksh[wid][row][hf]     = *(const float4*)kp;
-    *(float4*)&Ksh[wid][row][hf + 4] = *(const float4*)(kp + 4);
-    *(float4*)&Vsh[wid][row][hf]     = *(const float4*)vp;
-    *(float4*)&Vsh[wid][row][hf + 4] = *(const float4*)(vp + 4);
-    *(float4*)&Qsh[wid][row][hf]     = *(const float4*)qp;
-    *(float4*)&Qsh[wid][row][hf + 4] = *(const float4*)(qp + 4);
-    int g = lane >> 4, cc = lane & 15;
-    size_t ibase = ((size_t)bh * NCA + c) * 512;
-    float4 U  = *(const float4*)(init + ibase + lane * 4);
-    float4 T  = *(const float4*)(init + ibase + 256 + lane * 4);
-    float4 KV = *(const float4*)(kvtot + bh * 256 + lane * 4);
-    float om = 1.0f - rdec;
-    float geom = (om > 1e-8f) ? (1.0f - __expf(-inv_tau * (float)t0)) / om : (float)t0;
-    #pragma unroll 4
-    for (int s = 0; s < CHA; s++) {
-        int i = t0 + s;
-        geom = fmaf(geom, rdec, 1.0f);
-        float4 kf = *(const float4*)&Ksh[wid][s][4 * g];
-        float4 qf = *(const float4*)&Qsh[wid][s][4 * g];
-        float vv = Vsh[wid][s][cc];
-        float u0 = kf.x * vv, u1 = kf.y * vv, u2 = kf.z * vv, u3 = kf.w * vv;
-        U.x += u0; U.y += u1; U.z += u2; U.w += u3;
-        T.x = fmaf(rdec, T.x, u0); T.y = fmaf(rdec, T.y, u1);
-        T.z = fmaf(rdec, T.z, u2); T.w = fmaf(rdec, T.w, u3);
-        float p;
-        p = qf.x * (KV.x - U.x + T.x);
-        p = fmaf(qf.y, KV.y - U.y + T.y, p);
-        p = fmaf(qf.z, KV.z - U.z + T.z, p);
-        p = fmaf(qf.w, KV.w - U.w + T.w, p);
-        p += __shfl_xor(p, 16, 64);
-        p += __shfl_xor(p, 32, 64);
-        float deno = fmaxf((float)(Lseq - 1 - i) + geom, 1e-6f);
-        float yv = p * (0.25f / deno);
-        if (lane < 16) Ysh[wid][s][lane] = yv;
-    }
-    float* op = out + ((size_t)(b * Lseq + t0 + row)) * Dm + h * HDm + hf;
-    *(float4*)op       = *(const float4*)&Ysh[wid][row][hf];
-    *(float4*)(op + 4) = *(const float4*)&Ysh[wid][row][hf + 4];
+__global__ __launch_bounds__(256) void post2(const float* __restrict__ attn,
+                                             const float* __restrict__ o_w,
+                                             const float* __restrict__ o_b,
+                                             const float* __restrict__ yT,
+                                             const float* __restrict__ out_w,
+                                             float* __restrict__ cat2) {
+    __shared__ unsigned short As[64][40];
+    __shared__ unsigned short Ws[64][40];
+    int bx = blockIdx.x;
+    const float* A; const float* W; const float* bias; float* C;
+    int lda_m, lda_k, ldw, K, n0, m0;
+    if (bx < 256) {
+        A = attn; lda_m = 256; lda_k = 1; W = o_w; ldw = 256; bias = o_b;
+        C = cat2 + 256; K = 256;
+        n0 = (bx & 3) * 64; m0 = (bx >> 2) * 64;
+    } else {
+        int l = bx - 256;
+        A = yT; lda_m = 1; lda_k = Bsz * Lseq; W = out_w; ldw = DIm; bias = nullptr;
+        C = cat2; K = DIm;
+        n0 = (l & 3) * 64; m0 = (l >> 2) * 64;
+    }
+    int tid = threadIdx.x;
+    int wave = tid >> 6, lane = tid & 63;
+    int quad = lane >> 4, r = lane & 15;
+    int mo = (wave >> 1) * 32, no = (wave & 1) * 32;
+    f4v acc[2][2];
+    #pragma unroll
+    for (int i = 0; i < 2; i++)
+        #pragma unroll
+        for (int j = 0; j < 2; j++) acc[i][j] = (f4v){0.f, 0.f, 0.f, 0.f};
+    for (int k0 = 0; k0 < K; k0 += 32) {
+        if (lda_k == 1) {
+            int m = tid >> 2, kk = (tid & 3) * 8;
+            const float* ap = A + (size_t)(m0 + m) * lda_m + k0 + kk;
+            *(s8v*)&As[m][kk] = pack8(*(const float4*)ap, *(const float4*)(ap + 4));
+        } else {
+            int k = tid >> 3, m8 = (tid & 7) * 8;
+            const float* ap = A + (size_t)(k0 + k) * lda_k + m0 + m8;
+            float4 a0 = *(const float4*)ap;
+            float4 a1 = *(const float4*)(ap + 4);
+            float av[8] = {a0.x, a0.y, a0.z, a0.w, a1.x, a1.y, a1.z, a1.w};
+            #pragma unroll
+            for (int i = 0; i < 8; i++) As[m8 + i][k] = (unsigned short)f2bf(av[i]);
+        }
+        {
+            int n = tid >> 2, kk = (tid & 3) * 8;
+            const float* wp = W + (size_t)(n0 + n) * ldw + k0 + kk;
+            *(s8v*)&Ws[n][kk] = pack8(*(const float4*)wp, *(const float4*)(wp + 4));
+        }
+        __syncthreads();
+        s8v af[2], bf[2];
+        #pragma unroll
+        for (int i = 0; i < 2; i++) af[i] = *(const s8v*)&As[mo + i * 16 + r][quad * 8];
+        #pragma unroll
+        for (int j = 0; j < 2; j++) bf[j] = *(const s8v*)&Ws[no + j * 16 + r][quad * 8];
+        #pragma unroll
+        for (int i = 0; i < 2; i++)
+            #pragma unroll
+            for (int j = 0; j < 2; j++)
+                acc[i][j] = __builtin_amdgcn_mfma_f32_16x16x32_bf16(af[i], bf[j], acc[i][j], 0, 0, 0);
+        __syncthreads();
+    }
+    #pragma unroll
+    for (int i = 0; i < 2; i++)
+        #pragma unroll
+        for (int j = 0; j < 2; j++)
+            #pragma unroll
+            for (int reg = 0; reg < 4; reg++) {
+                int m = m0 + mo + i * 16 + quad * 4 + reg;
+                int n = n0 + no + j * 16 + r;
+                float v = acc[i][j][reg];
+                if (bias) v += bias[n];
+                C[(size_t)m * 512 + n] = v;
+            }
+}
+
+__global__ __launch_bounds__(256) void gate_gemm(const float* __restrict__ cat2,
+                                                 const float* __restrict__ gate_w,
+                                                 const float* __restrict__ gate_b,
+                                                 const float* __restrict__ xres,
+                                                 float* __restrict__ fout) {
+    __shared__ unsigned short As[64][40];
+    __shared__ unsigned short Ws[64][40];
+    int tid = threadIdx.x;
+    int wave = tid >> 6, lane = tid & 63;
+    int quad = lane >> 4, r = lane & 15;
+    int m0 = blockIdx.y * 64, n0 = blockIdx.x * 64;
+    int mo = (wave >> 1) * 32, no = (wave & 1) * 32;
+    f4v acc[2][2];
+    #pragma unroll
+    for (int i = 0; i < 2; i++)
+        #pragma unroll
+        for (int j = 0; j < 2; j++) acc[i][j] = (f4v){0.f, 0.f, 0.f, 0.f};
+    for (int k0 = 0; k0 < 512; k0 += 32) {
+        {
+            int m = tid >> 2, kk = (tid & 3) * 8;
+            const float* ap = cat2 + (size_t)(m0 + m) * 512 + k0 + kk;
+            *(s8v*)&As[m][kk] = pack8(*(const float4*)ap, *(const float4*)(ap + 4));
+        }
+        {
+            int n = tid >> 2, kk = (tid & 3) * 8;
+            const float* wp = gate_w + (size_t)(n0 + n) * 512 + k0 + kk;
+            *(s8v*)&Ws[n][kk] = pack8(*(const float4*)wp, *(const float4*)(wp + 4));
+        }
+        __syncthreads();
+        s8v af[2], bf[2];
+        #pragma unroll
+        for (int i = 0; i < 2; i++) af[i] = *(const s8v*)&As[mo + i * 16 + r][quad * 8];
+        #pragma unroll
+        for (int j = 0; j < 2; j++) bf[j] = *(const s8v*)&Ws[no + j * 16 + r][quad * 8];
+        #pragma unroll
+        for (int i = 0; i < 2; i++)
+            #pragma unroll
+            for (int j = 0; j < 2; j++)
+                acc[i][j] = __builtin_amdgcn_mfma_f32_16x16x32_bf16(af[i], bf[j], acc[i][j], 0, 0, 0);
+        __syncthreads();
+    }
+    #pragma unroll
+    for (int i = 0; i < 2; i++)
+        #pragma unroll
+        for (int j = 0; j < 2; j++)
+            #pragma unroll
+            for (int reg = 0; reg < 4; reg++) {
+                int m = m0 + mo + i * 16 + quad * 4 + reg;
+                int n = n0 + no + j * 16 + r;
+                float v = acc[i][j][reg] + gate_b[n];
+                float gg = 1.0f / (1.0f + __expf(-v));
+                float ssm = cat2[(size_t)m * 512 + n];
+                float ssd = cat2[(size_t)m * 512 + 256 + n];
+                fout[(size_t)m * 256 + n] = xres[(size_t)m * 256 + n] + gg * ssm + (1.0f - gg) * ssd;
+            }
 }
 
 extern "C" void kernel_launch(void* const* d_in, const int* in_sizes, int n_in,
@@ -808,41 +844,32 @@
     float* cat2  = ws + off; off += (size_t)M * 2 * Dm;
     float* xc    = cat2;
     float* q0    = qcat;
-
-    ln_kernel<<<M, 256, 0, stream>>>(x, ln_g, ln_b, xn);
-
-    halve3_kernel<<<(917504 + 255) / 256, 256, 0, stream>>>(xn, xd2, xd4, xd8);
+    float* loc   = xm;
+    float* kvtot = xd2;
+    float* hloc  = qcat;
+    float* Pc    = qcat + (size_t)NCH * NCHK * Ssz;
+
+    ln_pool<<<512, 256, 0, stream>>>(x, ln_g, ln_b, xn, xd2, xd4, xd8);
 
     proj8<<<2016, 256, 0, stream>>>(xn, xd2, xd4, xd8, in_proj_w,
         k_w, k_b, v_w, v_b, mq_w, mq_b,
         xm, zT, kmat, vmat, q0, qd2, qd4, qd8);
 
-    fuse_gemm<<<dim3(4, 64), 256, 0, stream>>>(q0, qd2, qd4, qd8, fuse_w, fuse_b, qbuf);
-
-    conv_silu_kernel<<<512, 256, 0, stream>>>(xm, conv_w, conv_b, xc, xcT);
-
-    gemm_bf16<<<dim3(3, 64), 256, 0, stream>>>(xc, DIm, 1, x_proj_w, DIm,
-        nullptr, dbc, 144, M, 144, DIm, 0, 0, nullptr, nullptr);
-
-    gemm_f32<<<dim3(8, 64), 256, 0, stream>>>(dbc, 144, 1, dt_w, DTRm,
-        dt_b, dtmT, M, M, DIm, DTRm, 1, 0, 1);
-
-    float* aloc  = qcat;
-    float* ainit = qcat + (size_t)64 * NCA * 512;
-    float* kvtot = qcat + (size_t)2 * 64 * NCA * 512;
-    attn_p1<<<512, 256, 0, stream>>>(kmat, vmat, log_tau, aloc);
-    attn_p2<<<64, 256, 0, stream>>>(aloc, log_tau, ainit, kvtot);
-    attn_p3<<<512, 256, 0, stream>>>(qbuf, kmat, vmat, log_tau, ainit, kvtot, attn);
-
-    float* hloc  = qcat;
-    float* Pc    = qcat + (size_t)NCH * NCHK * Ssz;
-    float* Hinit = qbuf;
-    scan_pass1<<<(NCH * NCHK) / 4, 256, 0, stream>>>(xcT, dtmT, dbc, A_log, hloc, Pc);
-    scan_combine<<<NCH / 4, 256, 0, stream>>>(hloc, Pc, Hinit);
-    scan_pass3<<<(NCH * NCHK) / 4, 256, 0, stream>>>(xcT, dtmT, zT, dbc, A_log, D_ssm, Hinit, yT);
+    mid2<<<768, 256, 0, stream>>>(q0, qd2, qd4, qd8, fuse_w, fuse_b, qbuf,
+        xm, conv_w, conv_b, xc, xcT);
+
+    xproj_ap1<<<1216, 256, 0, stream>>>(xc, x_proj_w, dbc, kmat, vmat, log_tau, loc);
+
+    dt_ap2<<<576, 256, 0, stream>>>(dbc, dt_w, dt_b, dtmT, loc, log_tau, kvtot);
+
+    sp1_ap3<<<9216, 256, 0, stream>>>(xcT, dtmT, dbc, A_log, hloc, Pc,
+        qbuf, kmat, vmat, log_tau, loc, kvtot, attn);
+
+    scan_combine<<<512, 256, 0, stream>>>(hloc, Pc);
+
+    scan_pass3<<<8192, 256, 0, stream>>>(xcT, dtmT, zT, dbc, A_log, D_ssm, hloc, yT);
 
     post2<<<512, 256, 0, stream>>>(attn, o_w, o_b, yT, out_w, cat2);
 
-    gemm_bf16<<<dim3(4, 64), 256, 0, stream>>>(cat2, 2 * Dm, 1, gate_w, 2 * Dm,
-        gate_b, nullptr, 0, M, Dm, 2 * Dm, 0, 0, x, outp);
-}
+    gate_gemm<<<dim3(4, 64), 256, 0, stream>>>(cat2, gate_w, gate_b, x, outp);
+}
```

Measured after the change: 321.5 us. 11.9% less time.
